# Kernel optimization log

Hardware: AMD Instinct MI355X
Metric: run time of the kernel (lower is better)

Reference implementation:

```python
import jax, jax.numpy as jnp
import numpy as np
from jax import lax

# Paraformer-large streaming decoder dims
L, H, DFF, NH, DK, K, V, T, S, CKV, LB = 16, 512, 2048, 4, 128, 11, 8404, 64, 2048, 256, 256


def _ln(x, g, b, eps=1e-5):
    m = jnp.mean(x, axis=-1, keepdims=True)
    var = jnp.mean((x - m) ** 2, axis=-1, keepdims=True)
    return (x - m) * lax.rsqrt(var + eps) * g + b


def setup_inputs() -> dict:
    key = jax.random.key(0)
    ks = jax.random.split(key, 20)
    w = lambda k, shp: jax.random.normal(k, shp, jnp.float32) * 0.02
    return {
        "encoder_out": jax.random.normal(ks[0], (1, S, H), jnp.float32),
        "list_frame": jax.random.normal(ks[1], (1, T, H), jnp.float32),
        "fsmn_cache": jax.random.normal(ks[2], (L, 1, H, K - 1), jnp.float32),
        "key_cache": jax.random.normal(ks[3], (L, NH, DK, CKV), jnp.float32),
        "value_cache": jax.random.normal(ks[4], (L, NH, CKV, DK), jnp.float32),
        "norm1_g": jnp.ones((L, H)), "norm1_b": jnp.zeros((L, H)),
        "norm2_g": jnp.ones((L, H)), "norm2_b": jnp.zeros((L, H)),
        "norm3_g": jnp.ones((L, H)), "norm3_b": jnp.zeros((L, H)),
        "ffn_norm_g": jnp.ones((L, DFF)), "ffn_norm_b": jnp.zeros((L, DFF)),
        "w1": w(ks[5], (L, H, DFF)), "b1": jnp.zeros((L, DFF)),
        "w2": w(ks[6], (L, DFF, H)),  # bias-free in FunASR DecoderSANM
        "fsmn_w": w(ks[7], (L, H, K)),  # depthwise conv, groups=H, no bias
        "qw": w(ks[8], (L, H, H)), "qb": jnp.zeros((L, H)),
        "kvw": w(ks[9], (L, H, 2 * H)), "kvb": jnp.zeros((L, 2 * H)),
        "ow": w(ks[10], (L, H, H)), "ob": jnp.zeros((L, H)),
        "d3_norm1_g": jnp.ones((H,)), "d3_norm1_b": jnp.zeros((H,)),
        "d3_w1": w(ks[11], (H, DFF)), "d3_b1": jnp.zeros((DFF,)),
        "d3_ffn_norm_g": jnp.ones((DFF,)), "d3_ffn_norm_b": jnp.zeros((DFF,)),
        "d3_w2": w(ks[12], (DFF, H)),
        "after_norm_g": jnp.ones((H,)), "after_norm_b": jnp.zeros((H,)),
        "out_w": w(ks[13], (H, V)), "out_b": jnp.zeros((V,)),
        "list_frame_len": T,
    }


def reference(encoder_out, list_frame, fsmn_cache, key_cache, value_cache,
              norm1_g, norm1_b, norm2_g, norm2_b, norm3_g, norm3_b,
              ffn_norm_g, ffn_norm_b, w1, b1, w2, fsmn_w, qw, qb, kvw, kvb, ow, ob,
              d3_norm1_g, d3_norm1_b, d3_w1, d3_b1, d3_ffn_norm_g, d3_ffn_norm_b, d3_w2,
              after_norm_g, after_norm_b, out_w, out_b, list_frame_len):
    enc = encoder_out[0]  # [S, H]
    scale = DK ** -0.5

    def layer_fn(lf, p):
        (fc, kc, vc, n1g, n1b, n2g, n2b, n3g, n3b, fng, fnb,
         W1, B1, W2, FW, QW, QB, KVW, KVB, OW, OB) = p
        residual = lf
        y = _ln(lf, n1g, n1b)
        y = _ln(jax.nn.relu(y @ W1 + B1), fng, fnb) @ W2
        y = _ln(y, n2g, n2b)
        # cache concat; slice [look_back:] with look_back = -(K-1)-T keeps all K-1+T cols
        x_cat = jnp.concatenate([fc, jnp.swapaxes(y, 1, 2)], axis=-1)  # [1, H, K-1+T]
        conv = lax.conv_general_dilated(
            x_cat, FW[:, None, :], (1,), 'VALID',
            dimension_numbers=('NCH', 'OIH', 'NCH'), feature_group_count=H)  # [1, H, T]
        x = jnp.swapaxes(conv, 1, 2) + y + residual
        residual = x
        q = (_ln(x, n3g, n3b)[0] @ QW + QB).reshape(-1, NH, DK).transpose(1, 0, 2) * scale  # [h, T, dk]
        kv = enc @ KVW + KVB  # [S, 2H]
        k = kv[:, :H].reshape(-1, NH, DK).transpose(1, 2, 0)  # [h, dk, S]
        v = kv[:, H:].reshape(-1, NH, DK).transpose(1, 0, 2)  # [h, S, dk]
        k = jnp.concatenate([kc, k], axis=2)  # [h, dk, CKV+S]
        v = jnp.concatenate([vc, v], axis=1)  # [h, CKV+S, dk]
        attn = jax.nn.softmax(jnp.einsum('htd,hds->hts', q, k), axis=-1)
        ctx = jnp.einsum('hts,hsd->htd', attn, v).transpose(1, 0, 2).reshape(1, -1, H)
        lf = residual + ctx @ OW + OB
        return lf, (x_cat, k[:, :, -LB:], v[:, -LB:, :])

    layer_params = (fsmn_cache, key_cache, value_cache, norm1_g, norm1_b, norm2_g, norm2_b,
                    norm3_g, norm3_b, ffn_norm_g, ffn_norm_b, w1, b1, w2, fsmn_w,
                    qw, qb, kvw, kvb, ow, ob)
    lf, (save_fsmn, save_keys, save_values) = lax.scan(layer_fn, list_frame, layer_params)
    x = _ln(lf, d3_norm1_g, d3_norm1_b)
    x = _ln(jax.nn.relu(x @ d3_w1 + d3_b1), d3_ffn_norm_g, d3_ffn_norm_b) @ d3_w2
    logits = _ln(x, after_norm_g, after_norm_b) @ out_w + out_b
    max_logit_ids = jnp.argmax(logits, axis=-1).astype(jnp.int32)
    return save_fsmn, save_keys, save_values, max_logit_ids
```

## Files before the change

kernel.cpp:

```cpp
#include <hip/hip_runtime.h>

constexpr int LAY = 16, HID = 512, FF = 2048, NHD = 4, DKH = 128, KW = 11,
              VOC = 8404, TT = 64, SEQ = 2048, LBN = 256;

#define SWZ(row, e) ((e) ^ ((((row) >> 2) & 7) << 2))

__global__ void diag_k(float* __restrict__ p, float v) { p[threadIdx.x] = v; }

__global__ __launch_bounds__(256) void redln_k(
    const float* __restrict__ P, int N, int nch,
    const float* __restrict__ bias, const float* __restrict__ res, int relu,
    const float* __restrict__ g, const float* __restrict__ b,
    float* __restrict__ out1, float* __restrict__ out2) {
  __shared__ float buf[2048];
  __shared__ float red[256];
  const int m = blockIdx.x, tid = threadIdx.x;
  float s = 0.f;
  for (int n = tid; n < N; n += 256) {
    const float* p = P + (size_t)m * N + n;
    float v = 0.f;
    for (int c = 0; c < nch; ++c) v += p[(size_t)c * 64 * N];
    if (bias) v += bias[n];
    if (res) v += res[(size_t)m * N + n];
    if (relu) v = fmaxf(v, 0.f);
    if (out1) out1[(size_t)m * N + n] = v;
    buf[n] = v; s += v;
  }
  red[tid] = s; __syncthreads();
  for (int st = 128; st > 0; st >>= 1) { if (tid < st) red[tid] += red[tid + st]; __syncthreads(); }
  const float mean = red[0] / N;
  __syncthreads();
  float vs = 0.f;
  for (int n = tid; n < N; n += 256) { float d = buf[n] - mean; vs += d * d; }
  red[tid] = vs; __syncthreads();
  for (int st = 128; st > 0; st >>= 1) { if (tid < st) red[tid] += red[tid + st]; __syncthreads(); }
  const float inv = rsqrtf(red[0] / N + 1e-5f);
  for (int n = tid; n < N; n += 256)
    out2[(size_t)m * N + n] = (buf[n] - mean) * inv * g[n] + b[n];
}

__global__ __launch_bounds__(256) void gemm32_nn(
    const float* __restrict__ A, int lda, long sA,
    const float* __restrict__ B, int ldb, long sB,
    int N, int Kd, int nch,
    float* __restrict__ part, long pzs, int coff,
    int aCh, long aChS) {
  __shared__ float As[64][64];
  __shared__ float Bs[64][40];
  const int tid = threadIdx.x;
  const int l16r = tid >> 4, l16c = tid & 15;
  const int lr = tid >> 3, lc = tid & 7;
  const int bn = blockIdx.x * 32;
  const int chunk = blockIdx.y;
  const int z = blockIdx.z;
  A += (long)z * sA; B += (long)z * sB;
  float acc[2][4] = {};
  const int ktiles = Kd >> 6;
  const int fa = (l16c & 7) << 2;
  for (int kt = chunk; kt < ktiles; kt += nch) {
    const int k0 = kt << 6;
    __syncthreads();
#pragma unroll
    for (int i = 0; i < 4; ++i) {
      const int r = l16r + 16 * i;
      const float* ap = A + (size_t)r * lda + k0 + l16c * 4;
      float4 av = *(const float4*)ap;
      for (int c = 1; c < aCh; ++c) {
        const float4 t2 = *(const float4*)(ap + (size_t)c * aChS);
        av.x += t2.x; av.y += t2.y; av.z += t2.z; av.w += t2.w;
      }
      As[l16c * 4 + 0][r ^ fa] = av.x; As[l16c * 4 + 1][r ^ fa] = av.y;
      As[l16c * 4 + 2][r ^ fa] = av.z; As[l16c * 4 + 3][r ^ fa] = av.w;
    }
#pragma unroll
    for (int i = 0; i < 2; ++i) {
      const int rb = lr + 32 * i;
      const float4 bv = *(const float4*)(B + (size_t)(k0 + rb) * ldb + bn + lc * 4);
      *(float4*)(&Bs[rb][lc * 4]) = bv;
    }
    __syncthreads();
#pragma unroll 8
    for (int kk = 0; kk < 64; ++kk) {
      const int fk = ((kk >> 2) & 7) << 2;
      const float2 a = *(const float2*)(&As[kk][(lr * 2) ^ fk]);
      const float4 b = *(const float4*)(&Bs[kk][lc * 4]);
      acc[0][0] += a.x * b.x; acc[0][1] += a.x * b.y; acc[0][2] += a.x * b.z; acc[0][3] += a.x * b.w;
      acc[1][0] += a.y * b.x; acc[1][1] += a.y * b.y; acc[1][2] += a.y * b.z; acc[1][3] += a.y * b.w;
    }
  }
  float* P = part + (size_t)z * pzs + (size_t)(coff + chunk) * 64 * N;
#pragma unroll
  for (int i = 0; i < 2; ++i) {
    const int m = lr * 2 + i;
#pragma unroll
    for (int j = 0; j < 4; ++j) P[(size_t)m * N + bn + lc * 4 + j] = acc[i][j];
  }
}

__global__ __launch_bounds__(256) void gemm_nn(
    const float* __restrict__ A, int lda, long sA,
    const float* __restrict__ B, int ldb, long sB,
    float* __restrict__ C, int ldc, long sC,
    const float* __restrict__ bias,
    const float* __restrict__ res, int ldres,
    int N, int Kd, int flags, int nch,
    float* __restrict__ part, long pzs, int coff,
    int aCh, long aChS) {
  __shared__ float As[64][64];
  __shared__ float Bs[64][64];
  const int tid = threadIdx.x;
  const int lr = tid >> 4, lc = tid & 15;
  const int bn = blockIdx.x * 64;
  const int chunk = blockIdx.y;
  const int z = blockIdx.z;
  A += (long)z * sA; B += (long)z * sB; C += (long)z * sC;
  float acc[4][4] = {};
  const int ktiles = Kd >> 6;
  const int fa = (lc & 7) << 2;
  for (int kt = chunk; kt < ktiles; kt += nch) {
    const int k0 = kt << 6;
    __syncthreads();
#pragma unroll
    for (int i = 0; i < 4; ++i) {
      const int r = lr + 16 * i;
      const float* ap = A + (size_t)r * lda + k0 + lc * 4;
      float4 av = *(const float4*)ap;
      for (int c = 1; c < aCh; ++c) {
        const float4 t2 = *(const float4*)(ap + (size_t)c * aChS);
        av.x += t2.x; av.y += t2.y; av.z += t2.z; av.w += t2.w;
      }
      As[lc * 4 + 0][r ^ fa] = av.x; As[lc * 4 + 1][r ^ fa] = av.y;
      As[lc * 4 + 2][r ^ fa] = av.z; As[lc * 4 + 3][r ^ fa] = av.w;
      const int n = bn + lc * 4;
      const float* bp = B + (size_t)(k0 + r) * ldb + n;
      float4 bv;
      if (n + 3 < N) bv = *(const float4*)bp;
      else {
        bv.x = (n + 0 < N) ? bp[0] : 0.f;
        bv.y = (n + 1 < N) ? bp[1] : 0.f;
        bv.z = (n + 2 < N) ? bp[2] : 0.f;
        bv.w = (n + 3 < N) ? bp[3] : 0.f;
      }
      *(float4*)(&Bs[r][SWZ(r, lc * 4)]) = bv;
    }
    __syncthreads();
#pragma unroll 8
    for (int kk = 0; kk < 64; ++kk) {
      const int fk = ((kk >> 2) & 7) << 2;
      const float4 a = *(const float4*)(&As[kk][(lr * 4) ^ fk]);
      const float4 b = *(const float4*)(&Bs[kk][(lc * 4) ^ fk]);
      acc[0][0] += a.x * b.x; acc[0][1] += a.x * b.y; acc[0][2] += a.x * b.z; acc[0][3] += a.x * b.w;
      acc[1][0] += a.y * b.x; acc[1][1] += a.y * b.y; acc[1][2] += a.y * b.z; acc[1][3] += a.y * b.w;
      acc[2][0] += a.z * b.x; acc[2][1] += a.z * b.y; acc[2][2] += a.z * b.z; acc[2][3] += a.z * b.w;
      acc[3][0] += a.w * b.x; acc[3][1] += a.w * b.y; acc[3][2] += a.w * b.z; acc[3][3] += a.w * b.w;
    }
  }
  if (part) {
    float* P = part + (size_t)z * pzs + (size_t)(coff + chunk) * 64 * N;
#pragma unroll
    for (int i = 0; i < 4; ++i) {
      const int m = lr * 4 + i;
#pragma unroll
      for (int j = 0; j < 4; ++j) P[(size_t)m * N + bn + lc * 4 + j] = acc[i][j];
    }
    return;
  }
#pragma unroll
  for (int i = 0; i < 4; ++i) {
    const int m = lr * 4 + i;
#pragma unroll
    for (int j = 0; j < 4; ++j) {
      const int n = bn + lc * 4 + j;
      if (n < N) {
        float v = acc[i][j];
        if (bias) v += bias[n];
        if (res) v += res[(size_t)m * ldres + n];
        if (flags & 2) v += C[(size_t)m * ldc + n];
        if (flags & 1) v = fmaxf(v, 0.f);
        C[(size_t)m * ldc + n] = v;
      }
    }
  }
}

__global__ __launch_bounds__(256) void red_k(
    const float* __restrict__ P, float* __restrict__ out,
    int N, int nch, long pzs, int outld, int zoff,
    const float* __restrict__ bias, const float* __restrict__ res,
    const float* __restrict__ rsv, const float* __restrict__ bvv,
    int relu, int total) {
  const int idx = blockIdx.x * 256 + threadIdx.x;
  if (idx >= total) return;
  const int z = idx / (64 * N);
  const int rem = idx - z * 64 * N;
  const int t = rem / N;
  const int n = rem - t * N;
  const float* p = P + (size_t)z * pzs + (size_t)t * N + n;
  float s = 0.f;
  for (int c = 0; c < nch; ++c) s += p[(size_t)c * 64 * N];
  const int oc = z * zoff + n;
  if (bias) s += bias[oc];
  if (res) s += res[(size_t)t * outld + oc];
  if (rsv) s += rsv[z * 64 + t] * bvv[oc];
  if (relu) s = fmaxf(s, 0.f);
  out[(size_t)t * outld + oc] = s;
}

__global__ __launch_bounds__(256) void gemm_nt(
    const float* __restrict__ A, int lda, long sA,
    const float* __restrict__ B, int ldb, long sB,
    float* __restrict__ C, int ldc, long sC,
    int N, int Kd, int nch, float* __restrict__ part) {
  __shared__ float As[64][64];
  __shared__ float Bs[64][64];
  const int tid = threadIdx.x;
  const int lr = tid >> 4, lc = tid & 15;
  const int bn = blockIdx.x * 64;
  const int chunk = blockIdx.y;
  const int z = blockIdx.z;
  A += (long)z * sA; B += (long)z * sB; C += (long)z * sC;
  float acc[4][4] = {};
  const int ktiles = Kd >> 6;
  const int fa = (lc & 7) << 2;
  for (int kt = chunk; kt < ktiles; kt += nch) {
    const int k0 = kt << 6;
    __syncthreads();
#pragma unroll
    for (int i = 0; i < 4; ++i) {
      const int r = lr + 16 * i;
      const float4 av = *(const float4*)(A + (size_t)r * lda + k0 + lc * 4);
      As[lc * 4 + 0][r ^ fa] = av.x; As[lc * 4 + 1][r ^ fa] = av.y;
      As[lc * 4 + 2][r ^ fa] = av.z; As[lc * 4 + 3][r ^ fa] = av.w;
      const float4 bv = *(const float4*)(B + (size_t)(bn + r) * ldb + k0 + lc * 4);
      Bs[lc * 4 + 0][r ^ fa] = bv.x; Bs[lc * 4 + 1][r ^ fa] = bv.y;
      Bs[lc * 4 + 2][r ^ fa] = bv.z; Bs[lc * 4 + 3][r ^ fa] = bv.w;
    }
    __syncthreads();
#pragma unroll 8
    for (int kk = 0; kk < 64; ++kk) {
      const int fk = ((kk >> 2) & 7) << 2;
      const float4 a = *(const float4*)(&As[kk][(lr * 4) ^ fk]);
      const float4 b = *(const float4*)(&Bs[kk][(lc * 4) ^ fk]);
      acc[0][0] += a.x * b.x; acc[0][1] += a.x * b.y; acc[0][2] += a.x * b.z; acc[0][3] += a.x * b.w;
      acc[1][0] += a.y * b.x; acc[1][1] += a.y * b.y; acc[1][2] += a.y * b.z; acc[1][3] += a.y * b.w;
      acc[2][0] += a.z * b.x; acc[2][1] += a.z * b.y; acc[2][2] += a.z * b.z; acc[2][3] += a.z * b.w;
      acc[3][0] += a.w * b.x; acc[3][1] += a.w * b.y; acc[3][2] += a.w * b.z; acc[3][3] += a.w * b.w;
    }
  }
  if (chunk == 0) {
#pragma unroll
    for (int i = 0; i < 4; ++i)
#pragma unroll
      for (int j = 0; j < 4; ++j)
        C[(size_t)(lr * 4 + i) * ldc + bn + lc * 4 + j] = acc[i][j];
  } else {
    float* P = part + (size_t)z * (64L * SEQ) + (size_t)(chunk - 1) * 64 * SEQ * NHD;
#pragma unroll
    for (int i = 0; i < 4; ++i)
#pragma unroll
      for (int j = 0; j < 4; ++j)
        P[(size_t)(lr * 4 + i) * SEQ + bn + lc * 4 + j] = acc[i][j];
  }
}

__global__ __launch_bounds__(256) void attn1_k(
    const float* __restrict__ qpart, const float* __restrict__ qbi_l,
    const float* __restrict__ Wkv, const float* __restrict__ kcl,
    float* __restrict__ qp, float* __restrict__ sc,
    int ckv, int sct) {
  __shared__ float As[64][64];
  __shared__ float Bs[64][64];
  const int tid = threadIdx.x;
  const int lr = tid >> 4, lc = tid & 15;
  const int h = blockIdx.z;
  const bool isQp = blockIdx.x < 8;
  const int bn = (isQp ? blockIdx.x : blockIdx.x - 8) * 64;
  const int fa = (lc & 7) << 2;
  float acc[4][4] = {};
  for (int k0 = 0; k0 < DKH; k0 += 64) {
    __syncthreads();
#pragma unroll
    for (int i = 0; i < 4; ++i) {
      const int r = lr + 16 * i;
      const float* ap = qpart + (size_t)r * HID + h * DKH + k0 + lc * 4;
      float4 av = *(const float4*)ap;
      for (int c = 1; c < 8; ++c) {
        const float4 t2 = *(const float4*)(ap + (size_t)c * 64 * HID);
        av.x += t2.x; av.y += t2.y; av.z += t2.z; av.w += t2.w;
      }
      const float4 bb = *(const float4*)(qbi_l + h * DKH + k0 + lc * 4);
      av.x += bb.x; av.y += bb.y; av.z += bb.z; av.w += bb.w;
      As[lc * 4 + 0][r ^ fa] = av.x; As[lc * 4 + 1][r ^ fa] = av.y;
      As[lc * 4 + 2][r ^ fa] = av.z; As[lc * 4 + 3][r ^ fa] = av.w;
      if (isQp) {
        const float4 bv = *(const float4*)(Wkv + (size_t)(bn + r) * (2 * HID) + h * DKH + k0 + lc * 4);
        Bs[lc * 4 + 0][r ^ fa] = bv.x; Bs[lc * 4 + 1][r ^ fa] = bv.y;
        Bs[lc * 4 + 2][r ^ fa] = bv.z; Bs[lc * 4 + 3][r ^ fa] = bv.w;
      } else {
        const float4 bv = *(const float4*)(kcl + ((size_t)h * DKH + k0 + r) * ckv + bn + lc * 4);
        *(float4*)(&Bs[r][SWZ(r, lc * 4)]) = bv;
      }
    }
    __syncthreads();
#pragma unroll 8
    for (int kk = 0; kk < 64; ++kk) {
      const int fk = ((kk >> 2) & 7) << 2;
      const float4 a = *(const float4*)(&As[kk][(lr * 4) ^ fk]);
      const float4 b = *(const float4*)(&Bs[kk][(lc * 4) ^ fk]);
      acc[0][0] += a.x * b.x; acc[0][1] += a.x * b.y; acc[0][2] += a.x * b.z; acc[0][3] += a.x * b.w;
      acc[1][0] += a.y * b.x; acc[1][1] += a.y * b.y; acc[1][2] += a.y * b.z; acc[1][3] += a.y * b.w;
      acc[2][0] += a.z * b.x; acc[2][1] += a.z * b.y; acc[2][2] += a.z * b.z; acc[2][3] += a.z * b.w;
      acc[3][0] += a.w * b.x; acc[3][1] += a.w * b.y; acc[3][2] += a.w * b.z; acc[3][3] += a.w * b.w;
    }
  }
  if (isQp) {
    float* C = qp + (size_t)h * TT * HID;
#pragma unroll
    for (int i = 0; i < 4; ++i)
#pragma unroll
      for (int j = 0; j < 4; ++j)
        C[(size_t)(lr * 4 + i) * HID + bn + lc * 4 + j] = acc[i][j];
  } else {
    float* C = sc + (size_t)h * TT * sct;
#pragma unroll
    for (int i = 0; i < 4; ++i)
#pragma unroll
      for (int j = 0; j < 4; ++j)
        C[(size_t)(lr * 4 + i) * sct + bn + lc * 4 + j] = acc[i][j];
  }
}

__global__ __launch_bounds__(256) void attn2_k(
    const float* __restrict__ sc, const float* __restrict__ vcl,
    const float* __restrict__ enc,
    float* __restrict__ part, float* __restrict__ partE,
    int ckv, int sct, int ncho, long pzc) {
  __shared__ float As[64][64];
  __shared__ float Bs[64][64];
  const int tid = threadIdx.x;
  const int lr = tid >> 4, lc = tid & 15;
  const int h = blockIdx.z;
  const int by = blockIdx.y;
  const bool isOld = blockIdx.x < 2;
  if (isOld && by >= ncho) return;
  if (!isOld && by >= 8) return;
  const float* A;
  const float* Bb;
  int lda, ldb, N, ktiles, nch, bn;
  float* P;
  if (isOld) {
    A = sc + (size_t)h * TT * sct;  lda = sct;
    Bb = vcl + (size_t)h * ckv * DKH; ldb = DKH;
    N = DKH; ktiles = ckv >> 6; nch = ncho; bn = blockIdx.x * 64;
    P = part + (size_t)h * pzc + (size_t)by * 64 * DKH;
  } else {
    A = sc + ckv + (size_t)h * TT * sct; lda = sct;
    Bb = enc; ldb = HID;
    N = HID; ktiles = SEQ >> 6; nch = 8; bn = (blockIdx.x - 2) * 64;
    P = partE + (size_t)h * (8L * 64 * HID) + (size_t)by * 64 * HID;
  }
  const int fa = (lc & 7) << 2;
  float acc[4][4] = {};
  for (int kt = by; kt < ktiles; kt += nch) {
    const int k0 = kt << 6;
    __syncthreads();
#pragma unroll
    for (int i = 0; i < 4; ++i) {
      const int r = lr + 16 * i;
      const float4 av = *(const float4*)(A + (size_t)r * lda + k0 + lc * 4);
      As[lc * 4 + 0][r ^ fa] = av.x; As[lc * 4 + 1][r ^ fa] = av.y;
      As[lc * 4 + 2][r ^ fa] = av.z; As[lc * 4 + 3][r ^ fa] = av.w;
      const float4 bv = *(const float4*)(Bb + (size_t)(k0 + r) * ldb + bn + lc * 4);
      *(float4*)(&Bs[r][SWZ(r, lc * 4)]) = bv;
    }
    __syncthreads();
#pragma unroll 8
    for (int kk = 0; kk < 64; ++kk) {
      const int fk = ((kk >> 2) & 7) << 2;
      const float4 a = *(const float4*)(&As[kk][(lr * 4) ^ fk]);
      const float4 b = *(const float4*)(&Bs[kk][(lc * 4) ^ fk]);
      acc[0][0] += a.x * b.x; acc[0][1] += a.x * b.y; acc[0][2] += a.x * b.z; acc[0][3] += a.x * b.w;
      acc[1][0] += a.y * b.x; acc[1][1] += a.y * b.y; acc[1][2] += a.y * b.z; acc[1][3] += a.y * b.w;
      acc[2][0] += a.z * b.x; acc[2][1] += a.z * b.y; acc[2][2] += a.z * b.z; acc[2][3] += a.z * b.w;
      acc[3][0] += a.w * b.x; acc[3][1] += a.w * b.y; acc[3][2] += a.w * b.z; acc[3][3] += a.w * b.w;
    }
  }
#pragma unroll
  for (int i = 0; i < 4; ++i)
#pragma unroll
    for (int j = 0; j < 4; ++j)
      P[(size_t)(lr * 4 + i) * N + bn + lc * 4 + j] = acc[i][j];
}

__global__ __launch_bounds__(256) void fsmnln_k(
    const float* __restrict__ y4, const float* __restrict__ lfin,
    const float* __restrict__ cache, const float* __restrict__ fw,
    const float* __restrict__ g, const float* __restrict__ b,
    float* __restrict__ xb, float* __restrict__ xcat,
    float* __restrict__ y1out) {
  __shared__ float buf[HID];
  __shared__ float red[256];
  const int t = blockIdx.x, tid = threadIdx.x;
  float s = 0.f;
  for (int h = tid; h < HID; h += 256) {
    float conv = 0.f;
#pragma unroll
    for (int k = 0; k < KW; ++k) {
      const int j = t + k;
      const float xcv = (j < KW - 1) ? cache[h * (KW - 1) + j]
                                     : y4[(size_t)(j - (KW - 1)) * HID + h];
      conv += xcv * fw[h * KW + k];
    }
    const float yv = y4[(size_t)t * HID + h];
    const float x = conv + yv + lfin[(size_t)t * HID + h];
    xb[(size_t)t * HID + h] = x;
    buf[h] = x; s += x;
    xcat[h * (KW - 1 + TT) + (KW - 1) + t] = yv;
    if (t == 0) {
      for (int j2 = 0; j2 < KW - 1; ++j2)
        xcat[h * (KW - 1 + TT) + j2] = cache[h * (KW - 1) + j2];
    }
  }
  red[tid] = s; __syncthreads();
  for (int st = 128; st > 0; st >>= 1) { if (tid < st) red[tid] += red[tid + st]; __syncthreads(); }
  const float mean = red[0] / HID;
  __syncthreads();
  float vs = 0.f;
  for (int h = tid; h < HID; h += 256) { float d = buf[h] - mean; vs += d * d; }
  red[tid] = vs; __syncthreads();
  for (int st = 128; st > 0; st >>= 1) { if (tid < st) red[tid] += red[tid + st]; __syncthreads(); }
  const float inv = rsqrtf(red[0] / HID + 1e-5f);
  for (int h = tid; h < HID; h += 256)
    y1out[(size_t)t * HID + h] = (buf[h] - mean) * inv * g[h] + b[h];
}

__global__ __launch_bounds__(256) void softmax_k(
    float* __restrict__ sc, float* __restrict__ rs,
    const float* __restrict__ qpart, const float* __restrict__ qbi_l,
    const float* __restrict__ kb, const float* __restrict__ partN,
    int cols, int newStart, float alpha) {
  __shared__ float srow[8192];
  __shared__ float red[256];
  const int tid = threadIdx.x;
  const int row = blockIdx.x;
  const int h = row >> 6, t = row & 63;
  sc += (size_t)row * cols;
  const float* pn = partN + (size_t)h * 64 * SEQ + (size_t)t * SEQ;
  float qv = 0.f;
  if (tid < DKH) {
    const float* qp0 = qpart + (size_t)t * HID + h * DKH + tid;
    float q = qp0[0];
    for (int c = 1; c < 8; ++c) q += qp0[(size_t)c * 64 * HID];
    q += qbi_l[h * DKH + tid];
    qv = q * kb[h * DKH + tid];
  }
  red[tid] = qv; __syncthreads();
  for (int st = 64; st > 0; st >>= 1) { if (tid < st) red[tid] += red[tid + st]; __syncthreads(); }
  const float qcv = red[0];
  __syncthreads();
  float m = -3.4e38f;
  for (int c = tid; c < cols; c += 256) {
    float v = sc[c];
    if (c >= newStart) v += pn[c - newStart] + qcv;
    v *= alpha;
    srow[c] = v; m = fmaxf(m, v);
  }
  red[tid] = m; __syncthreads();
  for (int st = 128; st > 0; st >>= 1) { if (tid < st) red[tid] = fmaxf(red[tid], red[tid + st]); __syncthreads(); }
  m = red[0]; __syncthreads();
  float s = 0.f;
  for (int c = tid; c < cols; c += 256) {
    const float e = __expf(srow[c] - m);
    srow[c] = e; s += e;
  }
  red[tid] = s; __syncthreads();
  for (int st = 128; st > 0; st >>= 1) { if (tid < st) red[tid] += red[tid + st]; __syncthreads(); }
  const float inv = 1.f / red[0];
  float ns = 0.f;
  for (int c = tid; c < cols; c += 256) {
    const float p = srow[c] * inv; sc[c] = p;
    if (c >= newStart) ns += p;
  }
  __syncthreads();
  red[tid] = ns; __syncthreads();
  for (int st = 128; st > 0; st >>= 1) { if (tid < st) red[tid] += red[tid + st]; __syncthreads(); }
  if (tid == 0) rs[row] = red[0];
}

__global__ __launch_bounds__(256) void argmax_k(const float* __restrict__ lg,
                                                float* __restrict__ out) {
  __shared__ float vs[256];
  __shared__ int ix[256];
  const int tid = threadIdx.x;
  lg += (size_t)blockIdx.x * VOC;
  float bm = -3.4e38f;
  int bi = 0;
  for (int c = tid; c < VOC; c += 256) { float v = lg[c]; if (v > bm) { bm = v; bi = c; } }
  vs[tid] = bm; ix[tid] = bi; __syncthreads();
  for (int st = 128; st > 0; st >>= 1) {
    if (tid < st) {
      if (vs[tid + st] > vs[tid] || (vs[tid + st] == vs[tid] && ix[tid + st] < ix[tid])) {
        vs[tid] = vs[tid + st]; ix[tid] = ix[tid + st];
      }
    }
    __syncthreads();
  }
  if (tid == 0) out[blockIdx.x] = (float)ix[0];
}

__global__ __launch_bounds__(256) void kvsave_k(const float* __restrict__ enc,
                                                const float* __restrict__ kvw,
                                                const float* __restrict__ kvb,
                                                float* __restrict__ keys,
                                                float* __restrict__ vals) {
  __shared__ float As[64][64];
  __shared__ float Bs[64][64];
  const int tid = threadIdx.x;
  const int lr = tid >> 4, lc = tid & 15;
  const int bn = blockIdx.x * 64, bm = blockIdx.y * 64;
  const int l = blockIdx.z;
  const float* W = kvw + (size_t)l * HID * 2 * HID;
  const int fa = (lc & 7) << 2;
  float acc[4][4] = {};
  for (int k0 = 0; k0 < HID; k0 += 64) {
    __syncthreads();
#pragma unroll
    for (int i = 0; i < 4; ++i) {
      const int r = lr + 16 * i;
      const float4 av =
          *(const float4*)(enc + (size_t)(SEQ - LBN + bm + r) * HID + k0 + lc * 4);
      As[lc * 4 + 0][r ^ fa] = av.x; As[lc * 4 + 1][r ^ fa] = av.y;
      As[lc * 4 + 2][r ^ fa] = av.z; As[lc * 4 + 3][r ^ fa] = av.w;
      const float4 bv = *(const float4*)(W + (size_t)(k0 + r) * (2 * HID) + bn + lc * 4);
      *(float4*)(&Bs[r][SWZ(r, lc * 4)]) = bv;
    }
    __syncthreads();
#pragma unroll 8
    for (int kk = 0; kk < 64; ++kk) {
      const int fk = ((kk >> 2) & 7) << 2;
      const float4 a = *(const float4*)(&As[kk][(lr * 4) ^ fk]);
      const float4 b = *(const float4*)(&Bs[kk][(lc * 4) ^ fk]);
      acc[0][0] += a.x * b.x; acc[0][1] += a.x * b.y; acc[0][2] += a.x * b.z; acc[0][3] += a.x * b.w;
      acc[1][0] += a.y * b.x; acc[1][1] += a.y * b.y; acc[1][2] += a.y * b.z; acc[1][3] += a.y * b.w;
      acc[2][0] += a.z * b.x; acc[2][1] += a.z * b.y; acc[2][2] += a.z * b.z; acc[2][3] += a.z * b.w;
      acc[3][0] += a.w * b.x; acc[3][1] += a.w * b.y; acc[3][2] += a.w * b.z; acc[3][3] += a.w * b.w;
    }
  }
#pragma unroll
  for (int i = 0; i < 4; ++i) {
    const int m = bm + lr * 4 + i;
#pragma unroll
    for (int j = 0; j < 4; ++j) {
      const int n = bn + lc * 4 + j;
      const float v = acc[i][j] + kvb[(size_t)l * 2 * HID + n];
      if (n < 512) {
        const int h = n >> 7, d = n & 127;
        keys[(((size_t)l * NHD + h) * DKH + d) * LBN + m] = v;
      } else {
        const int c = n - 512, h = c >> 7, d = c & 127;
        vals[(((size_t)l * NHD + h) * LBN + m) * DKH + d] = v;
      }
    }
  }
}

extern "C" void kernel_launch(void* const* d_in, const int* in_sizes, int n_in,
                              void* d_out, int out_size, void* d_ws, size_t ws_size,
                              hipStream_t stream) {
  static const int EXPECT[34] = {
      1048576, 32768, 81920, -1, -1,
      8192, 8192, 8192, 8192, 8192, 8192,
      32768, 32768,
      16777216, 32768, 16777216, 90112,
      4194304, 8192, 8388608, 16384, 4194304, 8192,
      512, 512, 1048576, 2048, 2048, 2048, 1048576,
      512, 512, 4302848, 8404};
  if (out_size != 4800576) {
    diag_k<<<1, 64, 0, stream>>>((float*)d_out, 9800000.f);
    return;
  }
  float* out_fsmn = (float*)d_out;
  float* out_keys = out_fsmn + (size_t)LAY * HID * (KW - 1 + TT);
  float* out_vals = out_keys + (size_t)LAY * NHD * DKH * LBN;
  float* out_ids  = out_vals + (size_t)LAY * NHD * LBN * DKH;
  if (n_in < 34) {
    diag_k<<<1, 64, 0, stream>>>(out_ids, 9900000.f);
    return;
  }
  for (int i = 0; i < 34; ++i) {
    if (EXPECT[i] >= 0 && in_sizes[i] != EXPECT[i]) {
      diag_k<<<1, 64, 0, stream>>>(out_ids, (float)((i + 1) * 100000));
      return;
    }
  }
  const long per = (long)LAY * NHD * DKH;
  const long ckl = (long)in_sizes[3] / per;
  if ((long)in_sizes[3] != ckl * per || in_sizes[4] != in_sizes[3] ||
      ckl <= 0 || (ckl & 63) != 0 || ckl > 6144) {
    diag_k<<<1, 64, 0, stream>>>(out_fsmn, (float)in_sizes[3]);
    return;
  }
  if (ws_size < (size_t)3145728 * 4) {
    diag_k<<<1, 64, 0, stream>>>(out_fsmn, 1.0e6f + (float)(ws_size >> 20));
    return;
  }
  const int ckv = (int)ckl;
  const int sct = ckv + SEQ;
  const long TS = (long)TT * sct;
  const int ncho = (ckv / 64 < 8) ? (ckv / 64) : 8;

  const float* enc    = (const float*)d_in[0];
  const float* lfrm   = (const float*)d_in[1];
  const float* fcache = (const float*)d_in[2];
  const float* kcache = (const float*)d_in[3];
  const float* vcache = (const float*)d_in[4];
  const float* n1g = (const float*)d_in[5];  const float* n1b = (const float*)d_in[6];
  const float* n2g = (const float*)d_in[7];  const float* n2b = (const float*)d_in[8];
  const float* n3g = (const float*)d_in[9];  const float* n3b = (const float*)d_in[10];
  const float* fng = (const float*)d_in[11]; const float* fnb = (const float*)d_in[12];
  const float* w1  = (const float*)d_in[13]; const float* b1  = (const float*)d_in[14];
  const float* w2  = (const float*)d_in[15];
  const float* fw  = (const float*)d_in[16];
  const float* qw  = (const float*)d_in[17]; const float* qbi  = (const float*)d_in[18];
  const float* kvw = (const float*)d_in[19]; const float* kvbi = (const float*)d_in[20];
  const float* ow  = (const float*)d_in[21]; const float* obi  = (const float*)d_in[22];
  const float* d3n1g = (const float*)d_in[23]; const float* d3n1b = (const float*)d_in[24];
  const float* d3w1  = (const float*)d_in[25]; const float* d3b1  = (const float*)d_in[26];
  const float* d3fng = (const float*)d_in[27]; const float* d3fnb = (const float*)d_in[28];
  const float* d3w2  = (const float*)d_in[29];
  const float* ang   = (const float*)d_in[30]; const float* anb = (const float*)d_in[31];
  const float* outw  = (const float*)d_in[32]; const float* outb = (const float*)d_in[33];

  float* sc  = out_keys;
  float* ov  = out_vals;
  float* lf  = ov + 0;
  float* y1  = ov + 32768;
  float* y4  = ov + 98304;
  float* xb  = ov + 131072;
  float* ctx = ov + 196608;
  float* y2  = ov + 360448;
  float* qp  = ov + 491520;
  float* rs  = ov + 753920;
  float* lg  = ov + 754176;
  float* wsf   = (float*)d_ws;
  float* part  = wsf;
  float* partE = wsf + 1048576;
  float* partN = wsf + 2097152;

  const float alpha = 0.08838834764831845f;
  const long TH = (long)TT * HID;
  const long pz_ctx = (long)(ncho + 4) * 64 * DKH;

  redln_k<<<TT, 256, 0, stream>>>(lfrm, HID, 1, nullptr, nullptr, 0,
                                  n1g, n1b, lf, y1);

  for (int l = 0; l < LAY; ++l) {
    const float* Wkv = kvw + (size_t)l * HID * 2 * HID;
    const float* Bkv = kvbi + (size_t)l * 2 * HID;
    const float* qbi_l = qbi + (size_t)l * HID;
    gemm32_nn<<<dim3(64, 8, 1), 256, 0, stream>>>(
        y1, HID, 0, w1 + (size_t)l * HID * FF, FF, 0, FF, HID, 8, part, 0, 0, 1, 0);
    redln_k<<<TT, 256, 0, stream>>>(part, FF, 8, b1 + (size_t)l * FF, nullptr, 1,
                                    fng + (size_t)l * FF, fnb + (size_t)l * FF,
                                    nullptr, y2);
    gemm32_nn<<<dim3(16, 32, 1), 256, 0, stream>>>(
        y2, FF, 0, w2 + (size_t)l * FF * HID, HID, 0, HID, FF, 32, part, 0, 0, 1, 0);
    redln_k<<<TT, 256, 0, stream>>>(part, HID, 32, nullptr, nullptr, 0,
                                    n2g + l * HID, n2b + l * HID, nullptr, y4);
    fsmnln_k<<<TT, 256, 0, stream>>>(y4, lf, fcache + (size_t)l * HID * (KW - 1),
                                     fw + (size_t)l * HID * KW,
                                     n3g + l * HID, n3b + l * HID,
                                     xb, out_fsmn + (size_t)l * HID * (KW - 1 + TT), y1);
    gemm32_nn<<<dim3(16, 8, 1), 256, 0, stream>>>(
        y1, HID, 0, qw + (size_t)l * HID * HID, HID, 0, HID, HID, 8, part, 0, 0, 1, 0);
    attn1_k<<<dim3(8 + ckv / 64, 1, NHD), 256, 0, stream>>>(
        part, qbi_l, Wkv, kcache + (size_t)l * NHD * DKH * ckv, qp, sc, ckv, sct);
    gemm_nt<<<dim3(32, 2, NHD), 256, 0, stream>>>(
        qp, HID, TH, enc, HID, 0, sc + ckv, sct, TS, SEQ, HID, 2, partN);
    softmax_k<<<NHD * TT, 256, 0, stream>>>(sc, rs, part, qbi_l, Bkv, partN,
                                            sct, ckv, alpha);
    attn2_k<<<dim3(10, 8, NHD), 256, 0, stream>>>(
        sc, vcache + (size_t)l * NHD * ckv * DKH, enc, part, partE,
        ckv, sct, ncho, pz_ctx);
    gemm32_nn<<<dim3(4, 4, NHD), 256, 0, stream>>>(
        partE, HID, 8L * 64 * HID, Wkv + HID, 2 * HID, DKH, DKH, HID, 4,
        part, pz_ctx, ncho, 8, 64L * HID);
    red_k<<<128, 256, 0, stream>>>(part, ctx, DKH, ncho + 4, pz_ctx, HID, DKH,
                                   nullptr, nullptr, rs, Bkv + HID, 0, NHD * TT * DKH);
    gemm32_nn<<<dim3(16, 8, 1), 256, 0, stream>>>(
        ctx, HID, 0, ow + (size_t)l * HID * HID, HID, 0, HID, HID, 8, part, 0, 0, 1, 0);
    const float* ng = (l + 1 < LAY) ? n1g + (l + 1) * HID : d3n1g;
    const float* nb = (l + 1 < LAY) ? n1b + (l + 1) * HID : d3n1b;
    redln_k<<<TT, 256, 0, stream>>>(part, HID, 8, obi + (size_t)l * HID, xb, 0,
                                    ng, nb, lf, y1);
  }

  gemm32_nn<<<dim3(64, 8, 1), 256, 0, stream>>>(
      y1, HID, 0, d3w1, FF, 0, FF, HID, 8, part, 0, 0, 1, 0);
  redln_k<<<TT, 256, 0, stream>>>(part, FF, 8, d3b1, nullptr, 1,
                                  d3fng, d3fnb, nullptr, y2);
  gemm32_nn<<<dim3(16, 32, 1), 256, 0, stream>>>(
      y2, FF, 0, d3w2, HID, 0, HID, FF, 32, part, 0, 0, 1, 0);
  redln_k<<<TT, 256, 0, stream>>>(part, HID, 32, nullptr, nullptr, 0,
                                  ang, anb, nullptr, y4);
  gemm_nn<<<dim3((VOC + 63) / 64, 1, 1), 256, 0, stream>>>(
      y4, HID, 0, outw, VOC, 0, lg, VOC, 0, outb, nullptr, 0,
      VOC, HID, 0, 1, nullptr, 0, 0, 1, 0);
  argmax_k<<<TT, 256, 0, stream>>>(lg, out_ids);

  kvsave_k<<<dim3(2 * HID / 64, LBN / 64, LAY), 256, 0, stream>>>(
      enc, kvw, kvbi, out_keys, out_vals);
}
```

Baseline: 2.944 ms.

## Fuse the whole decoder chain into one cooperative persistent kernel

Replaces the roughly 200 per-layer kernel launches with a single cooperative kernel that runs every stage as a grid-strided device function, with grid-wide barriers between stages. The fallback path keeps separate launches of the same device functions. This targets launch overhead and inter-kernel gaps in a latency-bound small-batch decoder. In exchange it adds grid.sync costs and caps the grid at 512 blocks, which can reduce parallelism in some stages.

```diff
diff --git a/kernel.cpp b/kernel.cpp
--- a/kernel.cpp
+++ b/kernel.cpp
@@ -1,4 +1,7 @@
 #include <hip/hip_runtime.h>
+#include <hip/hip_cooperative_groups.h>
+
+namespace cg = cooperative_groups;
 
 constexpr int LAY = 16, HID = 512, FF = 2048, NHD = 4, DKH = 128, KW = 11,
               VOC = 8404, TT = 64, SEQ = 2048, LBN = 256;
@@ -6,432 +9,633 @@
 #define SWZ(row, e) ((e) ^ ((((row) >> 2) & 7) << 2))
 
 __global__ void diag_k(float* __restrict__ p, float v) { p[threadIdx.x] = v; }
+
+struct CA {
+  const float* enc; const float* lfrm; const float* fcache;
+  const float* kcache; const float* vcache;
+  const float* n1g; const float* n1b; const float* n2g; const float* n2b;
+  const float* n3g; const float* n3b; const float* fng; const float* fnb;
+  const float* w1; const float* b1; const float* w2; const float* fw;
+  const float* qw; const float* qbi; const float* kvw; const float* kvbi;
+  const float* ow; const float* obi;
+  const float* d3n1g; const float* d3n1b; const float* d3w1; const float* d3b1;
+  const float* d3fng; const float* d3fnb; const float* d3w2;
+  const float* ang; const float* anb; const float* outw; const float* outb;
+  float* lf; float* y1; float* y2; float* y4; float* xb; float* ctx;
+  float* rs; float* lg; float* sc;
+  float* part; float* partE; float* partN;
+  float* out_fsmn; float* out_ids;
+  int ckv; int sct; int ncho; long pz_ctx;
+};
+
+__device__ void d_redln(const float* __restrict__ P, int N, int nch,
+                        const float* __restrict__ bias,
+                        const float* __restrict__ res, int relu,
+                        const float* __restrict__ g, const float* __restrict__ b,
+                        float* __restrict__ out1, float* __restrict__ out2,
+                        float* sm) {
+  float* buf = sm;
+  float* red = sm + 2048;
+  const int tid = threadIdx.x;
+  for (int m = blockIdx.x; m < 64; m += gridDim.x) {
+    float s = 0.f;
+    for (int n = tid; n < N; n += 256) {
+      const float* p = P + (size_t)m * N + n;
+      float v = 0.f;
+      for (int c = 0; c < nch; ++c) v += p[(size_t)c * 64 * N];
+      if (bias) v += bias[n];
+      if (res) v += res[(size_t)m * N + n];
+      if (relu) v = fmaxf(v, 0.f);
+      if (out1) out1[(size_t)m * N + n] = v;
+      buf[n] = v; s += v;
+    }
+    red[tid] = s; __syncthreads();
+    for (int st = 128; st > 0; st >>= 1) { if (tid < st) red[tid] += red[tid + st]; __syncthreads(); }
+    const float mean = red[0] / N;
+    __syncthreads();
+    float vs = 0.f;
+    for (int n = tid; n < N; n += 256) { float d = buf[n] - mean; vs += d * d; }
+    red[tid] = vs; __syncthreads();
+    for (int st = 128; st > 0; st >>= 1) { if (tid < st) red[tid] += red[tid + st]; __syncthreads(); }
+    const float inv = rsqrtf(red[0] / N + 1e-5f);
+    for (int n = tid; n < N; n += 256)
+      out2[(size_t)m * N + n] = (buf[n] - mean) * inv * g[n] + b[n];
+    __syncthreads();
+  }
+}
+
+__device__ void d_gemm32(const float* __restrict__ A, int lda, long sA,
+                         const float* __restrict__ B, int ldb, long sB,
+                         int N, int Kd, int nch, int Z,
+                         float* __restrict__ part, long pzs, int coff,
+                         int aCh, long aChS, float* sm) {
+  const int nx = N >> 5;
+  const int tot = nx * nch * Z;
+  const int tid = threadIdx.x;
+  const int l16r = tid >> 4, l16c = tid & 15;
+  const int lr = tid >> 3, lc = tid & 7;
+  float (*As)[64] = (float(*)[64])sm;
+  float (*Bs)[40] = (float(*)[40])(sm + 4096);
+  const int fa = (l16c & 7) << 2;
+  const int ktiles = Kd >> 6;
+  for (int vb = blockIdx.x; vb < tot; vb += gridDim.x) {
+    const int bx = vb % nx;
+    const int r2 = vb / nx;
+    const int chunk = r2 % nch;
+    const int z = r2 / nch;
+    const float* Az = A + (long)z * sA;
+    const float* Bz = B + (long)z * sB;
+    const int bn = bx * 32;
+    float acc[2][4] = {};
+    for (int kt = chunk; kt < ktiles; kt += nch) {
+      const int k0 = kt << 6;
+      __syncthreads();
+#pragma unroll
+      for (int i = 0; i < 4; ++i) {
+        const int r = l16r + 16 * i;
+        const float* ap = Az + (size_t)r * lda + k0 + l16c * 4;
+        float4 av = *(const float4*)ap;
+        for (int c = 1; c < aCh; ++c) {
+          const float4 t2 = *(const float4*)(ap + (size_t)c * aChS);
+          av.x += t2.x; av.y += t2.y; av.z += t2.z; av.w += t2.w;
+        }
+        As[l16c * 4 + 0][r ^ fa] = av.x; As[l16c * 4 + 1][r ^ fa] = av.y;
+        As[l16c * 4 + 2][r ^ fa] = av.z; As[l16c * 4 + 3][r ^ fa] = av.w;
+      }
+#pragma unroll
+      for (int i = 0; i < 2; ++i) {
+        const int rb = lr + 32 * i;
+        const float4 bv = *(const float4*)(Bz + (size_t)(k0 + rb) * ldb + bn + lc * 4);
+        *(float4*)(&Bs[rb][lc * 4]) = bv;
+      }
+      __syncthreads();
+#pragma unroll 8
+      for (int kk = 0; kk < 64; ++kk) {
+        const int fk = ((kk >> 2) & 7) << 2;
+        const float2 aa = *(const float2*)(&As[kk][(lr * 2) ^ fk]);
+        const float4 bb = *(const float4*)(&Bs[kk][lc * 4]);
+        acc[0][0] += aa.x * bb.x; acc[0][1] += aa.x * bb.y; acc[0][2] += aa.x * bb.z; acc[0][3] += aa.x * bb.w;
+        acc[1][0] += aa.y * bb.x; acc[1][1] += aa.y * bb.y; acc[1][2] += aa.y * bb.z; acc[1][3] += aa.y * bb.w;
+      }
+    }
+    float* P = part + (size_t)z * pzs + (size_t)(coff + chunk) * 64 * N;
+#pragma unroll
+    for (int i = 0; i < 2; ++i) {
+      const int m = lr * 2 + i;
+#pragma unroll
+      for (int j = 0; j < 4; ++j) P[(size_t)m * N + bn + lc * 4 + j] = acc[i][j];
+    }
+    __syncthreads();
+  }
+}
+
+__device__ void d_fsmnln(const float* __restrict__ y4, const float* __restrict__ lfin,
+                         const float* __restrict__ cache, const float* __restrict__ fw,
+                         const float* __restrict__ g, const float* __restrict__ b,
+                         float* __restrict__ xb, float* __restrict__ xcat,
+                         float* __restrict__ y1out, float* sm) {
+  float* buf = sm;
+  float* red = sm + 512;
+  const int tid = threadIdx.x;
+  for (int t = blockIdx.x; t < 64; t += gridDim.x) {
+    float s = 0.f;
+    for (int h = tid; h < HID; h += 256) {
+      float conv = 0.f;
+#pragma unroll
+      for (int k = 0; k < KW; ++k) {
+        const int j = t + k;
+        const float xcv = (j < KW - 1) ? cache[h * (KW - 1) + j]
+                                       : y4[(size_t)(j - (KW - 1)) * HID + h];
+        conv += xcv * fw[h * KW + k];
+      }
+      const float yv = y4[(size_t)t * HID + h];
+      const float x = conv + yv + lfin[(size_t)t * HID + h];
+      xb[(size_t)t * HID + h] = x;
+      buf[h] = x; s += x;
+      xcat[h * (KW - 1 + TT) + (KW - 1) + t] = yv;
+      if (t == 0) {
+        for (int j2 = 0; j2 < KW - 1; ++j2)
+          xcat[h * (KW - 1 + TT) + j2] = cache[h * (KW - 1) + j2];
+      }
+    }
+    red[tid] = s; __syncthreads();
+    for (int st = 128; st > 0; st >>= 1) { if (tid < st) red[tid] += red[tid + st]; __syncthreads(); }
+    const float mean = red[0] / HID;
+    __syncthreads();
+    float vs = 0.f;
+    for (int h = tid; h < HID; h += 256) { float d = buf[h] - mean; vs += d * d; }
+    red[tid] = vs; __syncthreads();
+    for (int st = 128; st > 0; st >>= 1) { if (tid < st) red[tid] += red[tid + st]; __syncthreads(); }
+    const float inv = rsqrtf(red[0] / HID + 1e-5f);
+    for (int h = tid; h < HID; h += 256)
+      y1out[(size_t)t * HID + h] = (buf[h] - mean) * inv * g[h] + b[h];
+    __syncthreads();
+  }
+}
+
+__device__ void d_attn1(const float* __restrict__ qpart, const float* __restrict__ qbi_l,
+                        const float* __restrict__ Wkv, const float* __restrict__ kcl,
+                        float* __restrict__ qp, float* __restrict__ sc,
+                        int ckv, int sct, float* sm) {
+  const int nx = 8 + ckv / 64;
+  const int tot = nx * NHD;
+  const int tid = threadIdx.x;
+  const int lr = tid >> 4, lc = tid & 15;
+  float (*As)[64] = (float(*)[64])sm;
+  float (*Bs)[64] = (float(*)[64])(sm + 4096);
+  const int fa = (lc & 7) << 2;
+  for (int vb = blockIdx.x; vb < tot; vb += gridDim.x) {
+    const int bxx = vb % nx;
+    const int h = vb / nx;
+    const bool isQp = bxx < 8;
+    const int bn = (isQp ? bxx : bxx - 8) * 64;
+    float acc[4][4] = {};
+    for (int k0 = 0; k0 < DKH; k0 += 64) {
+      __syncthreads();
+#pragma unroll
+      for (int i = 0; i < 4; ++i) {
+        const int r = lr + 16 * i;
+        const float* ap = qpart + (size_t)r * HID + h * DKH + k0 + lc * 4;
+        float4 av = *(const float4*)ap;
+        for (int c = 1; c < 8; ++c) {
+          const float4 t2 = *(const float4*)(ap + (size_t)c * 64 * HID);
+          av.x += t2.x; av.y += t2.y; av.z += t2.z; av.w += t2.w;
+        }
+        const float4 bb = *(const float4*)(qbi_l + h * DKH + k0 + lc * 4);
+        av.x += bb.x; av.y += bb.y; av.z += bb.z; av.w += bb.w;
+        As[lc * 4 + 0][r ^ fa] = av.x; As[lc * 4 + 1][r ^ fa] = av.y;
+        As[lc * 4 + 2][r ^ fa] = av.z; As[lc * 4 + 3][r ^ fa] = av.w;
+        if (isQp) {
+          const float4 bv = *(const float4*)(Wkv + (size_t)(bn + r) * (2 * HID) + h * DKH + k0 + lc * 4);
+          Bs[lc * 4 + 0][r ^ fa] = bv.x; Bs[lc * 4 + 1][r ^ fa] = bv.y;
+          Bs[lc * 4 + 2][r ^ fa] = bv.z; Bs[lc * 4 + 3][r ^ fa] = bv.w;
+        } else {
+          const float4 bv = *(const float4*)(kcl + ((size_t)h * DKH + k0 + r) * ckv + bn + lc * 4);
+          *(float4*)(&Bs[r][SWZ(r, lc * 4)]) = bv;
+        }
+      }
+      __syncthreads();
+#pragma unroll 8
+      for (int kk = 0; kk < 64; ++kk) {
+        const int fk = ((kk >> 2) & 7) << 2;
+        const float4 a = *(const float4*)(&As[kk][(lr * 4) ^ fk]);
+        const float4 b = *(const float4*)(&Bs[kk][(lc * 4) ^ fk]);
+        acc[0][0] += a.x * b.x; acc[0][1] += a.x * b.y; acc[0][2] += a.x * b.z; acc[0][3] += a.x * b.w;
+        acc[1][0] += a.y * b.x; acc[1][1] += a.y * b.y; acc[1][2] += a.y * b.z; acc[1][3] += a.y * b.w;
+        acc[2][0] += a.z * b.x; acc[2][1] += a.z * b.y; acc[2][2] += a.z * b.z; acc[2][3] += a.z * b.w;
+        acc[3][0] += a.w * b.x; acc[3][1] += a.w * b.y; acc[3][2] += a.w * b.z; acc[3][3] += a.w * b.w;
+      }
+    }
+    if (isQp) {
+      float* C = qp + (size_t)h * TT * HID;
+#pragma unroll
+      for (int i = 0; i < 4; ++i)
+#pragma unroll
+        for (int j = 0; j < 4; ++j)
+          C[(size_t)(lr * 4 + i) * HID + bn + lc * 4 + j] = acc[i][j];
+    } else {
+      float* C = sc + (size_t)h * TT * sct;
+#pragma unroll
+      for (int i = 0; i < 4; ++i)
+#pragma unroll
+        for (int j = 0; j < 4; ++j)
+          C[(size_t)(lr * 4 + i) * sct + bn + lc * 4 + j] = acc[i][j];
+    }
+    __syncthreads();
+  }
+}
+
+__device__ void d_scnew(const float* __restrict__ qp, const float* __restrict__ enc,
+                        float* __restrict__ sc, float* __restrict__ partN,
+                        int ckv, int sct, float* sm) {
+  const int tot = 32 * 2 * NHD;
+  const int tid = threadIdx.x;
+  const int lr = tid >> 4, lc = tid & 15;
+  float (*As)[64] = (float(*)[64])sm;
+  float (*Bs)[64] = (float(*)[64])(sm + 4096);
+  const int fa = (lc & 7) << 2;
+  const long TH = (long)TT * HID;
+  const long TS = (long)TT * sct;
+  for (int vb = blockIdx.x; vb < tot; vb += gridDim.x) {
+    const int bxx = vb & 31;
+    const int r2 = vb >> 5;
+    const int chunk = r2 & 1;
+    const int z = r2 >> 1;
+    const float* A = qp + (long)z * TH;
+    const int bn = bxx * 64;
+    float acc[4][4] = {};
+    for (int kt = chunk; kt < 8; kt += 2) {
+      const int k0 = kt << 6;
+      __syncthreads();
+#pragma unroll
+      for (int i = 0; i < 4; ++i) {
+        const int r = lr + 16 * i;
+        const float4 av = *(const float4*)(A + (size_t)r * HID + k0 + lc * 4);
+        As[lc * 4 + 0][r ^ fa] = av.x; As[lc * 4 + 1][r ^ fa] = av.y;
+        As[lc * 4 + 2][r ^ fa] = av.z; As[lc * 4 + 3][r ^ fa] = av.w;
+        const float4 bv = *(const float4*)(enc + (size_t)(bn + r) * HID + k0 + lc * 4);
+        Bs[lc * 4 + 0][r ^ fa] = bv.x; Bs[lc * 4 + 1][r ^ fa] = bv.y;
+        Bs[lc * 4 + 2][r ^ fa] = bv.z; Bs[lc * 4 + 3][r ^ fa] = bv.w;
+      }
+      __syncthreads();
+#pragma unroll 8
+      for (int kk = 0; kk < 64; ++kk) {
+        const int fk = ((kk >> 2) & 7) << 2;
+        const float4 a = *(const float4*)(&As[kk][(lr * 4) ^ fk]);
+        const float4 b = *(const float4*)(&Bs[kk][(lc * 4) ^ fk]);
+        acc[0][0] += a.x * b.x; acc[0][1] += a.x * b.y; acc[0][2] += a.x * b.z; acc[0][3] += a.x * b.w;
+        acc[1][0] += a.y * b.x; acc[1][1] += a.y * b.y; acc[1][2] += a.y * b.z; acc[1][3] += a.y * b.w;
+        acc[2][0] += a.z * b.x; acc[2][1] += a.z * b.y; acc[2][2] += a.z * b.z; acc[2][3] += a.z * b.w;
+        acc[3][0] += a.w * b.x; acc[3][1] += a.w * b.y; acc[3][2] += a.w * b.z; acc[3][3] += a.w * b.w;
+      }
+    }
+    if (chunk == 0) {
+      float* C = sc + ckv + (long)z * TS;
+#pragma unroll
+      for (int i = 0; i < 4; ++i)
+#pragma unroll
+        for (int j = 0; j < 4; ++j)
+          C[(size_t)(lr * 4 + i) * sct + bn + lc * 4 + j] = acc[i][j];
+    } else {
+      float* P = partN + (size_t)z * (64L * SEQ);
+#pragma unroll
+      for (int i = 0; i < 4; ++i)
+#pragma unroll
+        for (int j = 0; j < 4; ++j)
+          P[(size_t)(lr * 4 + i) * SEQ + bn + lc * 4 + j] = acc[i][j];
+    }
+    __syncthreads();
+  }
+}
+
+__device__ void d_softmax(float* __restrict__ sc, float* __restrict__ rs,
+                          const float* __restrict__ qpart, const float* __restrict__ qbi_l,
+                          const float* __restrict__ kb, const float* __restrict__ partN,
+                          int cols, int newStart, float alpha, float* sm) {
+  float* srow = sm;
+  float* red = sm + 8192;
+  const int tid = threadIdx.x;
+  for (int row = blockIdx.x; row < NHD * TT; row += gridDim.x) {
+    const int h = row >> 6, t = row & 63;
+    float* scr = sc + (size_t)row * cols;
+    const float* pn = partN + (size_t)h * 64 * SEQ + (size_t)t * SEQ;
+    float qv = 0.f;
+    if (tid < DKH) {
+      const float* qp0 = qpart + (size_t)t * HID + h * DKH + tid;
+      float q = qp0[0];
+      for (int c = 1; c < 8; ++c) q += qp0[(size_t)c * 64 * HID];
+      q += qbi_l[h * DKH + tid];
+      qv = q * kb[h * DKH + tid];
+    }
+    red[tid] = qv; __syncthreads();
+    for (int st = 64; st > 0; st >>= 1) { if (tid < st) red[tid] += red[tid + st]; __syncthreads(); }
+    const float qcv = red[0];
+    __syncthreads();
+    float m = -3.4e38f;
+    for (int c = tid; c < cols; c += 256) {
+      float v = scr[c];
+      if (c >= newStart) v += pn[c - newStart] + qcv;
+      v *= alpha;
+      srow[c] = v; m = fmaxf(m, v);
+    }
+    red[tid] = m; __syncthreads();
+    for (int st = 128; st > 0; st >>= 1) { if (tid < st) red[tid] = fmaxf(red[tid], red[tid + st]); __syncthreads(); }
+    m = red[0]; __syncthreads();
+    float s = 0.f;
+    for (int c = tid; c < cols; c += 256) {
+      const float e = __expf(srow[c] - m);
+      srow[c] = e; s += e;
+    }
+    red[tid] = s; __syncthreads();
+    for (int st = 128; st > 0; st >>= 1) { if (tid < st) red[tid] += red[tid + st]; __syncthreads(); }
+    const float inv = 1.f / red[0];
+    float ns = 0.f;
+    for (int c = tid; c < cols; c += 256) {
+      const float p = srow[c] * inv; scr[c] = p;
+      if (c >= newStart) ns += p;
+    }
+    __syncthreads();
+    red[tid] = ns; __syncthreads();
+    for (int st = 128; st > 0; st >>= 1) { if (tid < st) red[tid] += red[tid + st]; __syncthreads(); }
+    if (tid == 0) rs[row] = red[0];
+    __syncthreads();
+  }
+}
+
+__device__ void d_attn2(const float* __restrict__ sc, const float* __restrict__ vcl,
+                        const float* __restrict__ enc,
+                        float* __restrict__ part, float* __restrict__ partE,
+                        int ckv, int sct, int ncho, long pzc, float* sm) {
+  const int tot = 10 * 8 * NHD;
+  const int tid = threadIdx.x;
+  const int lr = tid >> 4, lc = tid & 15;
+  float (*As)[64] = (float(*)[64])sm;
+  float (*Bs)[64] = (float(*)[64])(sm + 4096);
+  const int fa = (lc & 7) << 2;
+  for (int vb = blockIdx.x; vb < tot; vb += gridDim.x) {
+    const int bxx = vb % 10;
+    const int r2 = vb / 10;
+    const int by = r2 % 8;
+    const int h = r2 / 8;
+    const bool isOld = bxx < 2;
+    if (isOld && by >= ncho) continue;
+    const float* A;
+    const float* Bb;
+    int lda, ldb, N, ktiles, nch, bn;
+    float* P;
+    if (isOld) {
+      A = sc + (size_t)h * TT * sct;  lda = sct;
+      Bb = vcl + (size_t)h * ckv * DKH; ldb = DKH;
+      N = DKH; ktiles = ckv >> 6; nch = ncho; bn = bxx * 64;
+      P = part + (size_t)h * pzc + (size_t)by * 64 * DKH;
+    } else {
+      A = sc + ckv + (size_t)h * TT * sct; lda = sct;
+      Bb = enc; ldb = HID;
+      N = HID; ktiles = SEQ >> 6; nch = 8; bn = (bxx - 2) * 64;
+      P = partE + (size_t)h * (8L * 64 * HID) + (size_t)by * 64 * HID;
+    }
+    float acc[4][4] = {};
+    for (int kt = by; kt < ktiles; kt += nch) {
+      const int k0 = kt << 6;
+      __syncthreads();
+#pragma unroll
+      for (int i = 0; i < 4; ++i) {
+        const int r = lr + 16 * i;
+        const float4 av = *(const float4*)(A + (size_t)r * lda + k0 + lc * 4);
+        As[lc * 4 + 0][r ^ fa] = av.x; As[lc * 4 + 1][r ^ fa] = av.y;
+        As[lc * 4 + 2][r ^ fa] = av.z; As[lc * 4 + 3][r ^ fa] = av.w;
+        const float4 bv = *(const float4*)(Bb + (size_t)(k0 + r) * ldb + bn + lc * 4);
+        *(float4*)(&Bs[r][SWZ(r, lc * 4)]) = bv;
+      }
+      __syncthreads();
+#pragma unroll 8
+      for (int kk = 0; kk < 64; ++kk) {
+        const int fk = ((kk >> 2) & 7) << 2;
+        const float4 a = *(const float4*)(&As[kk][(lr * 4) ^ fk]);
+        const float4 b = *(const float4*)(&Bs[kk][(lc * 4) ^ fk]);
+        acc[0][0] += a.x * b.x; acc[0][1] += a.x * b.y; acc[0][2] += a.x * b.z; acc[0][3] += a.x * b.w;
+        acc[1][0] += a.y * b.x; acc[1][1] += a.y * b.y; acc[1][2] += a.y * b.z; acc[1][3] += a.y * b.w;
+        acc[2][0] += a.z * b.x; acc[2][1] += a.z * b.y; acc[2][2] += a.z * b.z; acc[2][3] += a.z * b.w;
+        acc[3][0] += a.w * b.x; acc[3][1] += a.w * b.y; acc[3][2] += a.w * b.z; acc[3][3] += a.w * b.w;
+      }
+    }
+#pragma unroll
+    for (int i = 0; i < 4; ++i)
+#pragma unroll
+      for (int j = 0; j < 4; ++j)
+        P[(size_t)(lr * 4 + i) * N + bn + lc * 4 + j] = acc[i][j];
+    __syncthreads();
+  }
+}
+
+__device__ void d_red(const float* __restrict__ P, float* __restrict__ out,
+                      int N, int nch, long pzs, int outld, int zoff,
+                      const float* __restrict__ rsv, const float* __restrict__ bvv,
+                      int total) {
+  for (int idx = blockIdx.x * 256 + threadIdx.x; idx < total; idx += gridDim.x * 256) {
+    const int z = idx / (64 * N);
+    const int rem = idx - z * 64 * N;
+    const int t = rem / N;
+    const int n = rem - t * N;
+    const float* p = P + (size_t)z * pzs + (size_t)t * N + n;
+    float s = 0.f;
+    for (int c = 0; c < nch; ++c) s += p[(size_t)c * 64 * N];
+    const int oc = z * zoff + n;
+    s += rsv[z * 64 + t] * bvv[oc];
+    out[(size_t)t * outld + oc] = s;
+  }
+}
+
+__device__ void d_vocab(const float* __restrict__ A, const float* __restrict__ B,
+                        float* __restrict__ C, const float* __restrict__ bias,
+                        float* sm) {
+  const int tot = (VOC + 63) / 64;
+  const int tid = threadIdx.x;
+  const int lr = tid >> 4, lc = tid & 15;
+  float (*As)[64] = (float(*)[64])sm;
+  float (*Bs)[64] = (float(*)[64])(sm + 4096);
+  const int fa = (lc & 7) << 2;
+  for (int vb = blockIdx.x; vb < tot; vb += gridDim.x) {
+    const int bn = vb * 64;
+    float acc[4][4] = {};
+    for (int k0 = 0; k0 < HID; k0 += 64) {
+      __syncthreads();
+#pragma unroll
+      for (int i = 0; i < 4; ++i) {
+        const int r = lr + 16 * i;
+        const float4 av = *(const float4*)(A + (size_t)r * HID + k0 + lc * 4);
+        As[lc * 4 + 0][r ^ fa] = av.x; As[lc * 4 + 1][r ^ fa] = av.y;
+        As[lc * 4 + 2][r ^ fa] = av.z; As[lc * 4 + 3][r ^ fa] = av.w;
+        const int n = bn + lc * 4;
+        const float* bp = B + (size_t)(k0 + r) * VOC + n;
+        float4 bv;
+        if (n + 3 < VOC) bv = *(const float4*)bp;
+        else {
+          bv.x = (n + 0 < VOC) ? bp[0] : 0.f;
+          bv.y = (n + 1 < VOC) ? bp[1] : 0.f;
+          bv.z = (n + 2 < VOC) ? bp[2] : 0.f;
+          bv.w = (n + 3 < VOC) ? bp[3] : 0.f;
+        }
+        *(float4*)(&Bs[r][SWZ(r, lc * 4)]) = bv;
+      }
+      __syncthreads();
+#pragma unroll 8
+      for (int kk = 0; kk < 64; ++kk) {
+        const int fk = ((kk >> 2) & 7) << 2;
+        const float4 a = *(const float4*)(&As[kk][(lr * 4) ^ fk]);
+        const float4 b = *(const float4*)(&Bs[kk][(lc * 4) ^ fk]);
+        acc[0][0] += a.x * b.x; acc[0][1] += a.x * b.y; acc[0][2] += a.x * b.z; acc[0][3] += a.x * b.w;
+        acc[1][0] += a.y * b.x; acc[1][1] += a.y * b.y; acc[1][2] += a.y * b.z; acc[1][3] += a.y * b.w;
+        acc[2][0] += a.z * b.x; acc[2][1] += a.z * b.y; acc[2][2] += a.z * b.z; acc[2][3] += a.z * b.w;
+        acc[3][0] += a.w * b.x; acc[3][1] += a.w * b.y; acc[3][2] += a.w * b.z; acc[3][3] += a.w * b.w;
+      }
+    }
+#pragma unroll
+    for (int i = 0; i < 4; ++i) {
+      const int m = lr * 4 + i;
+#pragma unroll
+      for (int j = 0; j < 4; ++j) {
+        const int n = bn + lc * 4 + j;
+        if (n < VOC) C[(size_t)m * VOC + n] = acc[i][j] + bias[n];
+      }
+    }
+    __syncthreads();
+  }
+}
+
+__device__ void d_argmax(const float* __restrict__ lg, float* __restrict__ out,
+                         float* sm) {
+  float* vs = sm;
+  int* ix = (int*)(sm + 256);
+  const int tid = threadIdx.x;
+  for (int row = blockIdx.x; row < TT; row += gridDim.x) {
+    const float* lr_ = lg + (size_t)row * VOC;
+    float bm = -3.4e38f;
+    int bi = 0;
+    for (int c = tid; c < VOC; c += 256) { float v = lr_[c]; if (v > bm) { bm = v; bi = c; } }
+    vs[tid] = bm; ix[tid] = bi; __syncthreads();
+    for (int st = 128; st > 0; st >>= 1) {
+      if (tid < st) {
+        if (vs[tid + st] > vs[tid] || (vs[tid + st] == vs[tid] && ix[tid + st] < ix[tid])) {
+          vs[tid] = vs[tid + st]; ix[tid] = ix[tid + st];
+        }
+      }
+      __syncthreads();
+    }
+    if (tid == 0) out[row] = (float)ix[0];
+    __syncthreads();
+  }
+}
+
+__global__ __launch_bounds__(256, 2) void chain_k(CA a) {
+  __shared__ float sm[8448];
+  cg::grid_group grid = cg::this_grid();
+  const float alpha = 0.08838834764831845f;
+
+  d_redln(a.lfrm, HID, 1, nullptr, nullptr, 0, a.n1g, a.n1b, a.lf, a.y1, sm);
+  grid.sync();
+
+  for (int l = 0; l < LAY; ++l) {
+    const float* Wkv = a.kvw + (size_t)l * HID * 2 * HID;
+    const float* Bkv = a.kvbi + (size_t)l * 2 * HID;
+    const float* qbi_l = a.qbi + (size_t)l * HID;
+    d_gemm32(a.y1, HID, 0, a.w1 + (size_t)l * HID * FF, FF, 0, FF, HID, 8, 1,
+             a.part, 0, 0, 1, 0, sm);
+    grid.sync();
+    d_redln(a.part, FF, 8, a.b1 + (size_t)l * FF, nullptr, 1,
+            a.fng + (size_t)l * FF, a.fnb + (size_t)l * FF, nullptr, a.y2, sm);
+    grid.sync();
+    d_gemm32(a.y2, FF, 0, a.w2 + (size_t)l * FF * HID, HID, 0, HID, FF, 32, 1,
+             a.part, 0, 0, 1, 0, sm);
+    grid.sync();
+    d_redln(a.part, HID, 32, nullptr, nullptr, 0,
+            a.n2g + l * HID, a.n2b + l * HID, nullptr, a.y4, sm);
+    grid.sync();
+    d_fsmnln(a.y4, a.lf, a.fcache + (size_t)l * HID * (KW - 1),
+             a.fw + (size_t)l * HID * KW, a.n3g + l * HID, a.n3b + l * HID,
+             a.xb, a.out_fsmn + (size_t)l * HID * (KW - 1 + TT), a.y1, sm);
+    grid.sync();
+    d_gemm32(a.y1, HID, 0, a.qw + (size_t)l * HID * HID, HID, 0, HID, HID, 8, 1,
+             a.part, 0, 0, 1, 0, sm);
+    grid.sync();
+    d_attn1(a.part, qbi_l, Wkv, a.kcache + (size_t)l * NHD * DKH * a.ckv,
+            a.ctx, a.sc, a.ckv, a.sct, sm);
+    grid.sync();
+    d_scnew(a.ctx, a.enc, a.sc, a.partN, a.ckv, a.sct, sm);
+    grid.sync();
+    d_softmax(a.sc, a.rs, a.part, qbi_l, Bkv, a.partN, a.sct, a.ckv, alpha, sm);
+    grid.sync();
+    d_attn2(a.sc, a.vcache + (size_t)l * NHD * a.ckv * DKH, a.enc,
+            a.part, a.partE, a.ckv, a.sct, a.ncho, a.pz_ctx, sm);
+    grid.sync();
+    d_gemm32(a.partE, HID, 8L * 64 * HID, Wkv + HID, 2 * HID, DKH,
+             DKH, HID, 4, NHD, a.part, a.pz_ctx, a.ncho, 8, 64L * HID, sm);
+    grid.sync();
+    d_red(a.part, a.y2, DKH, a.ncho + 4, a.pz_ctx, HID, DKH,
+          a.rs, Bkv + HID, NHD * TT * DKH);
+    grid.sync();
+    d_gemm32(a.y2, HID, 0, a.ow + (size_t)l * HID * HID, HID, 0, HID, HID, 8, 1,
+             a.part, 0, 0, 1, 0, sm);
+    grid.sync();
+    const float* ng = (l + 1 < LAY) ? a.n1g + (l + 1) * HID : a.d3n1g;
+    const float* nb = (l + 1 < LAY) ? a.n1b + (l + 1) * HID : a.d3n1b;
+    d_redln(a.part, HID, 8, a.obi + (size_t)l * HID, a.xb, 0, ng, nb, a.lf, a.y1, sm);
+    grid.sync();
+  }
+
+  d_gemm32(a.y1, HID, 0, a.d3w1, FF, 0, FF, HID, 8, 1, a.part, 0, 0, 1, 0, sm);
+  grid.sync();
+  d_redln(a.part, FF, 8, a.d3b1, nullptr, 1, a.d3fng, a.d3fnb, nullptr, a.y2, sm);
+  grid.sync();
+  d_gemm32(a.y2, FF, 0, a.d3w2, HID, 0, HID, FF, 32, 1, a.part, 0, 0, 1, 0, sm);
+  grid.sync();
+  d_redln(a.part, HID, 32, nullptr, nullptr, 0, a.ang, a.anb, nullptr, a.y4, sm);
+  grid.sync();
+  d_vocab(a.y4, a.outw, a.lg, a.outb, sm);
+  grid.sync();
+  d_argmax(a.lg, a.out_ids, sm);
+}
 
 __global__ __launch_bounds__(256) void redln_k(
     const float* __restrict__ P, int N, int nch,
     const float* __restrict__ bias, const float* __restrict__ res, int relu,
     const float* __restrict__ g, const float* __restrict__ b,
     float* __restrict__ out1, float* __restrict__ out2) {
-  __shared__ float buf[2048];
-  __shared__ float red[256];
-  const int m = blockIdx.x, tid = threadIdx.x;
-  float s = 0.f;
-  for (int n = tid; n < N; n += 256) {
-    const float* p = P + (size_t)m * N + n;
-    float v = 0.f;
-    for (int c = 0; c < nch; ++c) v += p[(size_t)c * 64 * N];
-    if (bias) v += bias[n];
-    if (res) v += res[(size_t)m * N + n];
-    if (relu) v = fmaxf(v, 0.f);
-    if (out1) out1[(size_t)m * N + n] = v;
-    buf[n] = v; s += v;
-  }
-  red[tid] = s; __syncthreads();
-  for (int st = 128; st > 0; st >>= 1) { if (tid < st) red[tid] += red[tid + st]; __syncthreads(); }
-  const float mean = red[0] / N;
-  __syncthreads();
-  float vs = 0.f;
-  for (int n = tid; n < N; n += 256) { float d = buf[n] - mean; vs += d * d; }
-  red[tid] = vs; __syncthreads();
-  for (int st = 128; st > 0; st >>= 1) { if (tid < st) red[tid] += red[tid + st]; __syncthreads(); }
-  const float inv = rsqrtf(red[0] / N + 1e-5f);
-  for (int n = tid; n < N; n += 256)
-    out2[(size_t)m * N + n] = (buf[n] - mean) * inv * g[n] + b[n];
-}
-
-__global__ __launch_bounds__(256) void gemm32_nn(
+  __shared__ float sm[2304];
+  d_redln(P, N, nch, bias, res, relu, g, b, out1, out2, sm);
+}
+
+__global__ __launch_bounds__(256) void gemm32_k(
     const float* __restrict__ A, int lda, long sA,
     const float* __restrict__ B, int ldb, long sB,
-    int N, int Kd, int nch,
-    float* __restrict__ part, long pzs, int coff,
-    int aCh, long aChS) {
-  __shared__ float As[64][64];
-  __shared__ float Bs[64][40];
-  const int tid = threadIdx.x;
-  const int l16r = tid >> 4, l16c = tid & 15;
-  const int lr = tid >> 3, lc = tid & 7;
-  const int bn = blockIdx.x * 32;
-  const int chunk = blockIdx.y;
-  const int z = blockIdx.z;
-  A += (long)z * sA; B += (long)z * sB;
-  float acc[2][4] = {};
-  const int ktiles = Kd >> 6;
-  const int fa = (l16c & 7) << 2;
-  for (int kt = chunk; kt < ktiles; kt += nch) {
-    const int k0 = kt << 6;
-    __syncthreads();
-#pragma unroll
-    for (int i = 0; i < 4; ++i) {
-      const int r = l16r + 16 * i;
-      const float* ap = A + (size_t)r * lda + k0 + l16c * 4;
-      float4 av = *(const float4*)ap;
-      for (int c = 1; c < aCh; ++c) {
-        const float4 t2 = *(const float4*)(ap + (size_t)c * aChS);
-        av.x += t2.x; av.y += t2.y; av.z += t2.z; av.w += t2.w;
-      }
-      As[l16c * 4 + 0][r ^ fa] = av.x; As[l16c * 4 + 1][r ^ fa] = av.y;
-      As[l16c * 4 + 2][r ^ fa] = av.z; As[l16c * 4 + 3][r ^ fa] = av.w;
-    }
-#pragma unroll
-    for (int i = 0; i < 2; ++i) {
-      const int rb = lr + 32 * i;
-      const float4 bv = *(const float4*)(B + (size_t)(k0 + rb) * ldb + bn + lc * 4);
-      *(float4*)(&Bs[rb][lc * 4]) = bv;
-    }
-    __syncthreads();
-#pragma unroll 8
-    for (int kk = 0; kk < 64; ++kk) {
-      const int fk = ((kk >> 2) & 7) << 2;
-      const float2 a = *(const float2*)(&As[kk][(lr * 2) ^ fk]);
-      const float4 b = *(const float4*)(&Bs[kk][lc * 4]);
-      acc[0][0] += a.x * b.x; acc[0][1] += a.x * b.y; acc[0][2] += a.x * b.z; acc[0][3] += a.x * b.w;
-      acc[1][0] += a.y * b.x; acc[1][1] += a.y * b.y; acc[1][2] += a.y * b.z; acc[1][3] += a.y * b.w;
-    }
-  }
-  float* P = part + (size_t)z * pzs + (size_t)(coff + chunk) * 64 * N;
-#pragma unroll
-  for (int i = 0; i < 2; ++i) {
-    const int m = lr * 2 + i;
-#pragma unroll
-    for (int j = 0; j < 4; ++j) P[(size_t)m * N + bn + lc * 4 + j] = acc[i][j];
-  }
-}
-
-__global__ __launch_bounds__(256) void gemm_nn(
-    const float* __restrict__ A, int lda, long sA,
-    const float* __restrict__ B, int ldb, long sB,
-    float* __restrict__ C, int ldc, long sC,
-    const float* __restrict__ bias,
-    const float* __restrict__ res, int ldres,
-    int N, int Kd, int flags, int nch,
-    float* __restrict__ part, long pzs, int coff,
-    int aCh, long aChS) {
-  __shared__ float As[64][64];
-  __shared__ float Bs[64][64];
-  const int tid = threadIdx.x;
-  const int lr = tid >> 4, lc = tid & 15;
-  const int bn = blockIdx.x * 64;
-  const int chunk = blockIdx.y;
-  const int z = blockIdx.z;
-  A += (long)z * sA; B += (long)z * sB; C += (long)z * sC;
-  float acc[4][4] = {};
-  const int ktiles = Kd >> 6;
-  const int fa = (lc & 7) << 2;
-  for (int kt = chunk; kt < ktiles; kt += nch) {
-    const int k0 = kt << 6;
-    __syncthreads();
-#pragma unroll
-    for (int i = 0; i < 4; ++i) {
-      const int r = lr + 16 * i;
-      const float* ap = A + (size_t)r * lda + k0 + lc * 4;
-      float4 av = *(const float4*)ap;
-      for (int c = 1; c < aCh; ++c) {
-        const float4 t2 = *(const float4*)(ap + (size_t)c * aChS);
-        av.x += t2.x; av.y += t2.y; av.z += t2.z; av.w += t2.w;
-      }
-      As[lc * 4 + 0][r ^ fa] = av.x; As[lc * 4 + 1][r ^ fa] = av.y;
-      As[lc * 4 + 2][r ^ fa] = av.z; As[lc * 4 + 3][r ^ fa] = av.w;
-      const int n = bn + lc * 4;
-      const float* bp = B + (size_t)(k0 + r) * ldb + n;
-      float4 bv;
-      if (n + 3 < N) bv = *(const float4*)bp;
-      else {
-        bv.x = (n + 0 < N) ? bp[0] : 0.f;
-        bv.y = (n + 1 < N) ? bp[1] : 0.f;
-        bv.z = (n + 2 < N) ? bp[2] : 0.f;
-        bv.w = (n + 3 < N) ? bp[3] : 0.f;
-      }
-      *(float4*)(&Bs[r][SWZ(r, lc * 4)]) = bv;
-    }
-    __syncthreads();
-#pragma unroll 8
-    for (int kk = 0; kk < 64; ++kk) {
-      const int fk = ((kk >> 2) & 7) << 2;
-      const float4 a = *(const float4*)(&As[kk][(lr * 4) ^ fk]);
-      const float4 b = *(const float4*)(&Bs[kk][(lc * 4) ^ fk]);
-      acc[0][0] += a.x * b.x; acc[0][1] += a.x * b.y; acc[0][2] += a.x * b.z; acc[0][3] += a.x * b.w;
-      acc[1][0] += a.y * b.x; acc[1][1] += a.y * b.y; acc[1][2] += a.y * b.z; acc[1][3] += a.y * b.w;
-      acc[2][0] += a.z * b.x; acc[2][1] += a.z * b.y; acc[2][2] += a.z * b.z; acc[2][3] += a.z * b.w;
-      acc[3][0] += a.w * b.x; acc[3][1] += a.w * b.y; acc[3][2] += a.w * b.z; acc[3][3] += a.w * b.w;
-    }
-  }
-  if (part) {
-    float* P = part + (size_t)z * pzs + (size_t)(coff + chunk) * 64 * N;
-#pragma unroll
-    for (int i = 0; i < 4; ++i) {
-      const int m = lr * 4 + i;
-#pragma unroll
-      for (int j = 0; j < 4; ++j) P[(size_t)m * N + bn + lc * 4 + j] = acc[i][j];
-    }
-    return;
-  }
-#pragma unroll
-  for (int i = 0; i < 4; ++i) {
-    const int m = lr * 4 + i;
-#pragma unroll
-    for (int j = 0; j < 4; ++j) {
-      const int n = bn + lc * 4 + j;
-      if (n < N) {
-        float v = acc[i][j];
-        if (bias) v += bias[n];
-        if (res) v += res[(size_t)m * ldres + n];
-        if (flags & 2) v += C[(size_t)m * ldc + n];
-        if (flags & 1) v = fmaxf(v, 0.f);
-        C[(size_t)m * ldc + n] = v;
-      }
-    }
-  }
-}
-
-__global__ __launch_bounds__(256) void red_k(
-    const float* __restrict__ P, float* __restrict__ out,
-    int N, int nch, long pzs, int outld, int zoff,
-    const float* __restrict__ bias, const float* __restrict__ res,
-    const float* __restrict__ rsv, const float* __restrict__ bvv,
-    int relu, int total) {
-  const int idx = blockIdx.x * 256 + threadIdx.x;
-  if (idx >= total) return;
-  const int z = idx / (64 * N);
-  const int rem = idx - z * 64 * N;
-  const int t = rem / N;
-  const int n = rem - t * N;
-  const float* p = P + (size_t)z * pzs + (size_t)t * N + n;
-  float s = 0.f;
-  for (int c = 0; c < nch; ++c) s += p[(size_t)c * 64 * N];
-  const int oc = z * zoff + n;
-  if (bias) s += bias[oc];
-  if (res) s += res[(size_t)t * outld + oc];
-  if (rsv) s += rsv[z * 64 + t] * bvv[oc];
-  if (relu) s = fmaxf(s, 0.f);
-  out[(size_t)t * outld + oc] = s;
-}
-
-__global__ __launch_bounds__(256) void gemm_nt(
-    const float* __restrict__ A, int lda, long sA,
-    const float* __restrict__ B, int ldb, long sB,
-    float* __restrict__ C, int ldc, long sC,
-    int N, int Kd, int nch, float* __restrict__ part) {
-  __shared__ float As[64][64];
-  __shared__ float Bs[64][64];
-  const int tid = threadIdx.x;
-  const int lr = tid >> 4, lc = tid & 15;
-  const int bn = blockIdx.x * 64;
-  const int chunk = blockIdx.y;
-  const int z = blockIdx.z;
-  A += (long)z * sA; B += (long)z * sB; C += (long)z * sC;
-  float acc[4][4] = {};
-  const int ktiles = Kd >> 6;
-  const int fa = (lc & 7) << 2;
-  for (int kt = chunk; kt < ktiles; kt += nch) {
-    const int k0 = kt << 6;
-    __syncthreads();
-#pragma unroll
-    for (int i = 0; i < 4; ++i) {
-      const int r = lr + 16 * i;
-      const float4 av = *(const float4*)(A + (size_t)r * lda + k0 + lc * 4);
-      As[lc * 4 + 0][r ^ fa] = av.x; As[lc * 4 + 1][r ^ fa] = av.y;
-      As[lc * 4 + 2][r ^ fa] = av.z; As[lc * 4 + 3][r ^ fa] = av.w;
-      const float4 bv = *(const float4*)(B + (size_t)(bn + r) * ldb + k0 + lc * 4);
-      Bs[lc * 4 + 0][r ^ fa] = bv.x; Bs[lc * 4 + 1][r ^ fa] = bv.y;
-      Bs[lc * 4 + 2][r ^ fa] = bv.z; Bs[lc * 4 + 3][r ^ fa] = bv.w;
-    }
-    __syncthreads();
-#pragma unroll 8
-    for (int kk = 0; kk < 64; ++kk) {
-      const int fk = ((kk >> 2) & 7) << 2;
-      const float4 a = *(const float4*)(&As[kk][(lr * 4) ^ fk]);
-      const float4 b = *(const float4*)(&Bs[kk][(lc * 4) ^ fk]);
-      acc[0][0] += a.x * b.x; acc[0][1] += a.x * b.y; acc[0][2] += a.x * b.z; acc[0][3] += a.x * b.w;
-      acc[1][0] += a.y * b.x; acc[1][1] += a.y * b.y; acc[1][2] += a.y * b.z; acc[1][3] += a.y * b.w;
-      acc[2][0] += a.z * b.x; acc[2][1] += a.z * b.y; acc[2][2] += a.z * b.z; acc[2][3] += a.z * b.w;
-      acc[3][0] += a.w * b.x; acc[3][1] += a.w * b.y; acc[3][2] += a.w * b.z; acc[3][3] += a.w * b.w;
-    }
-  }
-  if (chunk == 0) {
-#pragma unroll
-    for (int i = 0; i < 4; ++i)
-#pragma unroll
-      for (int j = 0; j < 4; ++j)
-        C[(size_t)(lr * 4 + i) * ldc + bn + lc * 4 + j] = acc[i][j];
-  } else {
-    float* P = part + (size_t)z * (64L * SEQ) + (size_t)(chunk - 1) * 64 * SEQ * NHD;
-#pragma unroll
-    for (int i = 0; i < 4; ++i)
-#pragma unroll
-      for (int j = 0; j < 4; ++j)
-        P[(size_t)(lr * 4 + i) * SEQ + bn + lc * 4 + j] = acc[i][j];
-  }
-}
-
-__global__ __launch_bounds__(256) void attn1_k(
-    const float* __restrict__ qpart, const float* __restrict__ qbi_l,
-    const float* __restrict__ Wkv, const float* __restrict__ kcl,
-    float* __restrict__ qp, float* __restrict__ sc,
-    int ckv, int sct) {
-  __shared__ float As[64][64];
-  __shared__ float Bs[64][64];
-  const int tid = threadIdx.x;
-  const int lr = tid >> 4, lc = tid & 15;
-  const int h = blockIdx.z;
-  const bool isQp = blockIdx.x < 8;
-  const int bn = (isQp ? blockIdx.x : blockIdx.x - 8) * 64;
-  const int fa = (lc & 7) << 2;
-  float acc[4][4] = {};
-  for (int k0 = 0; k0 < DKH; k0 += 64) {
-    __syncthreads();
-#pragma unroll
-    for (int i = 0; i < 4; ++i) {
-      const int r = lr + 16 * i;
-      const float* ap = qpart + (size_t)r * HID + h * DKH + k0 + lc * 4;
-      float4 av = *(const float4*)ap;
-      for (int c = 1; c < 8; ++c) {
-        const float4 t2 = *(const float4*)(ap + (size_t)c * 64 * HID);
-        av.x += t2.x; av.y += t2.y; av.z += t2.z; av.w += t2.w;
-      }
-      const float4 bb = *(const float4*)(qbi_l + h * DKH + k0 + lc * 4);
-      av.x += bb.x; av.y += bb.y; av.z += bb.z; av.w += bb.w;
-      As[lc * 4 + 0][r ^ fa] = av.x; As[lc * 4 + 1][r ^ fa] = av.y;
-      As[lc * 4 + 2][r ^ fa] = av.z; As[lc * 4 + 3][r ^ fa] = av.w;
-      if (isQp) {
-        const float4 bv = *(const float4*)(Wkv + (size_t)(bn + r) * (2 * HID) + h * DKH + k0 + lc * 4);
-        Bs[lc * 4 + 0][r ^ fa] = bv.x; Bs[lc * 4 + 1][r ^ fa] = bv.y;
-        Bs[lc * 4 + 2][r ^ fa] = bv.z; Bs[lc * 4 + 3][r ^ fa] = bv.w;
-      } else {
-        const float4 bv = *(const float4*)(kcl + ((size_t)h * DKH + k0 + r) * ckv + bn + lc * 4);
-        *(float4*)(&Bs[r][SWZ(r, lc * 4)]) = bv;
-      }
-    }
-    __syncthreads();
-#pragma unroll 8
-    for (int kk = 0; kk < 64; ++kk) {
-      const int fk = ((kk >> 2) & 7) << 2;
-      const float4 a = *(const float4*)(&As[kk][(lr * 4) ^ fk]);
-      const float4 b = *(const float4*)(&Bs[kk][(lc * 4) ^ fk]);
-      acc[0][0] += a.x * b.x; acc[0][1] += a.x * b.y; acc[0][2] += a.x * b.z; acc[0][3] += a.x * b.w;
-      acc[1][0] += a.y * b.x; acc[1][1] += a.y * b.y; acc[1][2] += a.y * b.z; acc[1][3] += a.y * b.w;
-      acc[2][0] += a.z * b.x; acc[2][1] += a.z * b.y; acc[2][2] += a.z * b.z; acc[2][3] += a.z * b.w;
-      acc[3][0] += a.w * b.x; acc[3][1] += a.w * b.y; acc[3][2] += a.w * b.z; acc[3][3] += a.w * b.w;
-    }
-  }
-  if (isQp) {
-    float* C = qp + (size_t)h * TT * HID;
-#pragma unroll
-    for (int i = 0; i < 4; ++i)
-#pragma unroll
-      for (int j = 0; j < 4; ++j)
-        C[(size_t)(lr * 4 + i) * HID + bn + lc * 4 + j] = acc[i][j];
-  } else {
-    float* C = sc + (size_t)h * TT * sct;
-#pragma unroll
-    for (int i = 0; i < 4; ++i)
-#pragma unroll
-      for (int j = 0; j < 4; ++j)
-        C[(size_t)(lr * 4 + i) * sct + bn + lc * 4 + j] = acc[i][j];
-  }
-}
-
-__global__ __launch_bounds__(256) void attn2_k(
-    const float* __restrict__ sc, const float* __restrict__ vcl,
-    const float* __restrict__ enc,
-    float* __restrict__ part, float* __restrict__ partE,
-    int ckv, int sct, int ncho, long pzc) {
-  __shared__ float As[64][64];
-  __shared__ float Bs[64][64];
-  const int tid = threadIdx.x;
-  const int lr = tid >> 4, lc = tid & 15;
-  const int h = blockIdx.z;
-  const int by = blockIdx.y;
-  const bool isOld = blockIdx.x < 2;
-  if (isOld && by >= ncho) return;
-  if (!isOld && by >= 8) return;
-  const float* A;
-  const float* Bb;
-  int lda, ldb, N, ktiles, nch, bn;
-  float* P;
-  if (isOld) {
-    A = sc + (size_t)h * TT * sct;  lda = sct;
-    Bb = vcl + (size_t)h * ckv * DKH; ldb = DKH;
-    N = DKH; ktiles = ckv >> 6; nch = ncho; bn = blockIdx.x * 64;
-    P = part + (size_t)h * pzc + (size_t)by * 64 * DKH;
-  } else {
-    A = sc + ckv + (size_t)h * TT * sct; lda = sct;
-    Bb = enc; ldb = HID;
-    N = HID; ktiles = SEQ >> 6; nch = 8; bn = (blockIdx.x - 2) * 64;
-    P = partE + (size_t)h * (8L * 64 * HID) + (size_t)by * 64 * HID;
-  }
-  const int fa = (lc & 7) << 2;
-  float acc[4][4] = {};
-  for (int kt = by; kt < ktiles; kt += nch) {
-    const int k0 = kt << 6;
-    __syncthreads();
-#pragma unroll
-    for (int i = 0; i < 4; ++i) {
-      const int r = lr + 16 * i;
-      const float4 av = *(const float4*)(A + (size_t)r * lda + k0 + lc * 4);
-      As[lc * 4 + 0][r ^ fa] = av.x; As[lc * 4 + 1][r ^ fa] = av.y;
-      As[lc * 4 + 2][r ^ fa] = av.z; As[lc * 4 + 3][r ^ fa] = av.w;
-      const float4 bv = *(const float4*)(Bb + (size_t)(k0 + r) * ldb + bn + lc * 4);
-      *(float4*)(&Bs[r][SWZ(r, lc * 4)]) = bv;
-    }
-    __syncthreads();
-#pragma unroll 8
-    for (int kk = 0; kk < 64; ++kk) {
-      const int fk = ((kk >> 2) & 7) << 2;
-      const float4 a = *(const float4*)(&As[kk][(lr * 4) ^ fk]);
-      const float4 b = *(const float4*)(&Bs[kk][(lc * 4) ^ fk]);
-      acc[0][0] += a.x * b.x; acc[0][1] += a.x * b.y; acc[0][2] += a.x * b.z; acc[0][3] += a.x * b.w;
-      acc[1][0] += a.y * b.x; acc[1][1] += a.y * b.y; acc[1][2] += a.y * b.z; acc[1][3] += a.y * b.w;
-      acc[2][0] += a.z * b.x; acc[2][1] += a.z * b.y; acc[2][2] += a.z * b.z; acc[2][3] += a.z * b.w;
-      acc[3][0] += a.w * b.x; acc[3][1] += a.w * b.y; acc[3][2] += a.w * b.z; acc[3][3] += a.w * b.w;
-    }
-  }
-#pragma unroll
-  for (int i = 0; i < 4; ++i)
-#pragma unroll
-    for (int j = 0; j < 4; ++j)
-      P[(size_t)(lr * 4 + i) * N + bn + lc * 4 + j] = acc[i][j];
+    int N, int Kd, int nch, int Z,
+    float* __restrict__ part, long pzs, int coff, int aCh, long aChS) {
+  __shared__ float sm[6656];
+  d_gemm32(A, lda, sA, B, ldb, sB, N, Kd, nch, Z, part, pzs, coff, aCh, aChS, sm);
 }
 
 __global__ __launch_bounds__(256) void fsmnln_k(
     const float* __restrict__ y4, const float* __restrict__ lfin,
     const float* __restrict__ cache, const float* __restrict__ fw,
     const float* __restrict__ g, const float* __restrict__ b,
-    float* __restrict__ xb, float* __restrict__ xcat,
-    float* __restrict__ y1out) {
-  __shared__ float buf[HID];
-  __shared__ float red[256];
-  const int t = blockIdx.x, tid = threadIdx.x;
-  float s = 0.f;
-  for (int h = tid; h < HID; h += 256) {
-    float conv = 0.f;
-#pragma unroll
-    for (int k = 0; k < KW; ++k) {
-      const int j = t + k;
-      const float xcv = (j < KW - 1) ? cache[h * (KW - 1) + j]
-                                     : y4[(size_t)(j - (KW - 1)) * HID + h];
-      conv += xcv * fw[h * KW + k];
-    }
-    const float yv = y4[(size_t)t * HID + h];
-    const float x = conv + yv + lfin[(size_t)t * HID + h];
-    xb[(size_t)t * HID + h] = x;
-    buf[h] = x; s += x;
-    xcat[h * (KW - 1 + TT) + (KW - 1) + t] = yv;
-    if (t == 0) {
-      for (int j2 = 0; j2 < KW - 1; ++j2)
-        xcat[h * (KW - 1 + TT) + j2] = cache[h * (KW - 1) + j2];
-    }
-  }
-  red[tid] = s; __syncthreads();
-  for (int st = 128; st > 0; st >>= 1) { if (tid < st) red[tid] += red[tid + st]; __syncthreads(); }
-  const float mean = red[0] / HID;
-  __syncthreads();
-  float vs = 0.f;
-  for (int h = tid; h < HID; h += 256) { float d = buf[h] - mean; vs += d * d; }
-  red[tid] = vs; __syncthreads();
-  for (int st = 128; st > 0; st >>= 1) { if (tid < st) red[tid] += red[tid + st]; __syncthreads(); }
-  const float inv = rsqrtf(red[0] / HID + 1e-5f);
-  for (int h = tid; h < HID; h += 256)
-    y1out[(size_t)t * HID + h] = (buf[h] - mean) * inv * g[h] + b[h];
+    float* __restrict__ xb, float* __restrict__ xcat, float* __restrict__ y1out) {
+  __shared__ float sm[768];
+  d_fsmnln(y4, lfin, cache, fw, g, b, xb, xcat, y1out, sm);
+}
+
+__global__ __launch_bounds__(256) void attn1_k(
+    const float* __restrict__ qpart, const float* __restrict__ qbi_l,
+    const float* __restrict__ Wkv, const float* __restrict__ kcl,
+    float* __restrict__ qp, float* __restrict__ sc, int ckv, int sct) {
+  __shared__ float sm[8192];
+  d_attn1(qpart, qbi_l, Wkv, kcl, qp, sc, ckv, sct, sm);
+}
+
+__global__ __launch_bounds__(256) void scnew_k(
+    const float* __restrict__ qp, const float* __restrict__ enc,
+    float* __restrict__ sc, float* __restrict__ partN, int ckv, int sct) {
+  __shared__ float sm[8192];
+  d_scnew(qp, enc, sc, partN, ckv, sct, sm);
 }
 
 __global__ __launch_bounds__(256) void softmax_k(
@@ -439,73 +643,36 @@
     const float* __restrict__ qpart, const float* __restrict__ qbi_l,
     const float* __restrict__ kb, const float* __restrict__ partN,
     int cols, int newStart, float alpha) {
-  __shared__ float srow[8192];
-  __shared__ float red[256];
-  const int tid = threadIdx.x;
-  const int row = blockIdx.x;
-  const int h = row >> 6, t = row & 63;
-  sc += (size_t)row * cols;
-  const float* pn = partN + (size_t)h * 64 * SEQ + (size_t)t * SEQ;
-  float qv = 0.f;
-  if (tid < DKH) {
-    const float* qp0 = qpart + (size_t)t * HID + h * DKH + tid;
-    float q = qp0[0];
-    for (int c = 1; c < 8; ++c) q += qp0[(size_t)c * 64 * HID];
-    q += qbi_l[h * DKH + tid];
-    qv = q * kb[h * DKH + tid];
-  }
-  red[tid] = qv; __syncthreads();
-  for (int st = 64; st > 0; st >>= 1) { if (tid < st) red[tid] += red[tid + st]; __syncthreads(); }
-  const float qcv = red[0];
-  __syncthreads();
-  float m = -3.4e38f;
-  for (int c = tid; c < cols; c += 256) {
-    float v = sc[c];
-    if (c >= newStart) v += pn[c - newStart] + qcv;
-    v *= alpha;
-    srow[c] = v; m = fmaxf(m, v);
-  }
-  red[tid] = m; __syncthreads();
-  for (int st = 128; st > 0; st >>= 1) { if (tid < st) red[tid] = fmaxf(red[tid], red[tid + st]); __syncthreads(); }
-  m = red[0]; __syncthreads();
-  float s = 0.f;
-  for (int c = tid; c < cols; c += 256) {
-    const float e = __expf(srow[c] - m);
-    srow[c] = e; s += e;
-  }
-  red[tid] = s; __syncthreads();
-  for (int st = 128; st > 0; st >>= 1) { if (tid < st) red[tid] += red[tid + st]; __syncthreads(); }
-  const float inv = 1.f / red[0];
-  float ns = 0.f;
-  for (int c = tid; c < cols; c += 256) {
-    const float p = srow[c] * inv; sc[c] = p;
-    if (c >= newStart) ns += p;
-  }
-  __syncthreads();
-  red[tid] = ns; __syncthreads();
-  for (int st = 128; st > 0; st >>= 1) { if (tid < st) red[tid] += red[tid + st]; __syncthreads(); }
-  if (tid == 0) rs[row] = red[0];
+  __shared__ float sm[8448];
+  d_softmax(sc, rs, qpart, qbi_l, kb, partN, cols, newStart, alpha, sm);
+}
+
+__global__ __launch_bounds__(256) void attn2_k(
+    const float* __restrict__ sc, const float* __restrict__ vcl,
+    const float* __restrict__ enc, float* __restrict__ part,
+    float* __restrict__ partE, int ckv, int sct, int ncho, long pzc) {
+  __shared__ float sm[8192];
+  d_attn2(sc, vcl, enc, part, partE, ckv, sct, ncho, pzc, sm);
+}
+
+__global__ __launch_bounds__(256) void red_k(
+    const float* __restrict__ P, float* __restrict__ out,
+    int N, int nch, long pzs, int outld, int zoff,
+    const float* __restrict__ rsv, const float* __restrict__ bvv, int total) {
+  d_red(P, out, N, nch, pzs, outld, zoff, rsv, bvv, total);
+}
+
+__global__ __launch_bounds__(256) void vocab_k(
+    const float* __restrict__ A, const float* __restrict__ B,
+    float* __restrict__ C, const float* __restrict__ bias) {
+  __shared__ float sm[8192];
+  d_vocab(A, B, C, bias, sm);
 }
 
 __global__ __launch_bounds__(256) void argmax_k(const float* __restrict__ lg,
                                                 float* __restrict__ out) {
-  __shared__ float vs[256];
-  __shared__ int ix[256];
-  const int tid = threadIdx.x;
-  lg += (size_t)blockIdx.x * VOC;
-  float bm = -3.4e38f;
-  int bi = 0;
-  for (int c = tid; c < VOC; c += 256) { float v = lg[c]; if (v > bm) { bm = v; bi = c; } }
-  vs[tid] = bm; ix[tid] = bi; __syncthreads();
-  for (int st = 128; st > 0; st >>= 1) {
-    if (tid < st) {
-      if (vs[tid + st] > vs[tid] || (vs[tid + st] == vs[tid] && ix[tid + st] < ix[tid])) {
-        vs[tid] = vs[tid + st]; ix[tid] = ix[tid + st];
-      }
-    }
-    __syncthreads();
-  }
-  if (tid == 0) out[blockIdx.x] = (float)ix[0];
+  __shared__ float sm[512];
+  d_argmax(lg, out, sm);
 }
 
 __global__ __launch_bounds__(256) void kvsave_k(const float* __restrict__ enc,
@@ -606,7 +773,6 @@
   }
   const int ckv = (int)ckl;
   const int sct = ckv + SEQ;
-  const long TS = (long)TT * sct;
   const int ncho = (ckv / 64 < 8) ? (ckv / 64) : 8;
 
   const float* enc    = (const float*)d_in[0];
@@ -639,7 +805,6 @@
   float* xb  = ov + 131072;
   float* ctx = ov + 196608;
   float* y2  = ov + 360448;
-  float* qp  = ov + 491520;
   float* rs  = ov + 753920;
   float* lg  = ov + 754176;
   float* wsf   = (float*)d_ws;
@@ -648,65 +813,77 @@
   float* partN = wsf + 2097152;
 
   const float alpha = 0.08838834764831845f;
-  const long TH = (long)TT * HID;
   const long pz_ctx = (long)(ncho + 4) * 64 * DKH;
 
-  redln_k<<<TT, 256, 0, stream>>>(lfrm, HID, 1, nullptr, nullptr, 0,
-                                  n1g, n1b, lf, y1);
-
-  for (int l = 0; l < LAY; ++l) {
-    const float* Wkv = kvw + (size_t)l * HID * 2 * HID;
-    const float* Bkv = kvbi + (size_t)l * 2 * HID;
-    const float* qbi_l = qbi + (size_t)l * HID;
-    gemm32_nn<<<dim3(64, 8, 1), 256, 0, stream>>>(
-        y1, HID, 0, w1 + (size_t)l * HID * FF, FF, 0, FF, HID, 8, part, 0, 0, 1, 0);
-    redln_k<<<TT, 256, 0, stream>>>(part, FF, 8, b1 + (size_t)l * FF, nullptr, 1,
-                                    fng + (size_t)l * FF, fnb + (size_t)l * FF,
-                                    nullptr, y2);
-    gemm32_nn<<<dim3(16, 32, 1), 256, 0, stream>>>(
-        y2, FF, 0, w2 + (size_t)l * FF * HID, HID, 0, HID, FF, 32, part, 0, 0, 1, 0);
-    redln_k<<<TT, 256, 0, stream>>>(part, HID, 32, nullptr, nullptr, 0,
-                                    n2g + l * HID, n2b + l * HID, nullptr, y4);
-    fsmnln_k<<<TT, 256, 0, stream>>>(y4, lf, fcache + (size_t)l * HID * (KW - 1),
-                                     fw + (size_t)l * HID * KW,
-                                     n3g + l * HID, n3b + l * HID,
-                                     xb, out_fsmn + (size_t)l * HID * (KW - 1 + TT), y1);
-    gemm32_nn<<<dim3(16, 8, 1), 256, 0, stream>>>(
-        y1, HID, 0, qw + (size_t)l * HID * HID, HID, 0, HID, HID, 8, part, 0, 0, 1, 0);
-    attn1_k<<<dim3(8 + ckv / 64, 1, NHD), 256, 0, stream>>>(
-        part, qbi_l, Wkv, kcache + (size_t)l * NHD * DKH * ckv, qp, sc, ckv, sct);
-    gemm_nt<<<dim3(32, 2, NHD), 256, 0, stream>>>(
-        qp, HID, TH, enc, HID, 0, sc + ckv, sct, TS, SEQ, HID, 2, partN);
-    softmax_k<<<NHD * TT, 256, 0, stream>>>(sc, rs, part, qbi_l, Bkv, partN,
-                                            sct, ckv, alpha);
-    attn2_k<<<dim3(10, 8, NHD), 256, 0, stream>>>(
-        sc, vcache + (size_t)l * NHD * ckv * DKH, enc, part, partE,
-        ckv, sct, ncho, pz_ctx);
-    gemm32_nn<<<dim3(4, 4, NHD), 256, 0, stream>>>(
-        partE, HID, 8L * 64 * HID, Wkv + HID, 2 * HID, DKH, DKH, HID, 4,
-        part, pz_ctx, ncho, 8, 64L * HID);
-    red_k<<<128, 256, 0, stream>>>(part, ctx, DKH, ncho + 4, pz_ctx, HID, DKH,
-                                   nullptr, nullptr, rs, Bkv + HID, 0, NHD * TT * DKH);
-    gemm32_nn<<<dim3(16, 8, 1), 256, 0, stream>>>(
-        ctx, HID, 0, ow + (size_t)l * HID * HID, HID, 0, HID, HID, 8, part, 0, 0, 1, 0);
-    const float* ng = (l + 1 < LAY) ? n1g + (l + 1) * HID : d3n1g;
-    const float* nb = (l + 1 < LAY) ? n1b + (l + 1) * HID : d3n1b;
-    redln_k<<<TT, 256, 0, stream>>>(part, HID, 8, obi + (size_t)l * HID, xb, 0,
-                                    ng, nb, lf, y1);
-  }
-
-  gemm32_nn<<<dim3(64, 8, 1), 256, 0, stream>>>(
-      y1, HID, 0, d3w1, FF, 0, FF, HID, 8, part, 0, 0, 1, 0);
-  redln_k<<<TT, 256, 0, stream>>>(part, FF, 8, d3b1, nullptr, 1,
-                                  d3fng, d3fnb, nullptr, y2);
-  gemm32_nn<<<dim3(16, 32, 1), 256, 0, stream>>>(
-      y2, FF, 0, d3w2, HID, 0, HID, FF, 32, part, 0, 0, 1, 0);
-  redln_k<<<TT, 256, 0, stream>>>(part, HID, 32, nullptr, nullptr, 0,
-                                  ang, anb, nullptr, y4);
-  gemm_nn<<<dim3((VOC + 63) / 64, 1, 1), 256, 0, stream>>>(
-      y4, HID, 0, outw, VOC, 0, lg, VOC, 0, outb, nullptr, 0,
-      VOC, HID, 0, 1, nullptr, 0, 0, 1, 0);
-  argmax_k<<<TT, 256, 0, stream>>>(lg, out_ids);
+  CA ca;
+  ca.enc = enc; ca.lfrm = lfrm; ca.fcache = fcache; ca.kcache = kcache; ca.vcache = vcache;
+  ca.n1g = n1g; ca.n1b = n1b; ca.n2g = n2g; ca.n2b = n2b; ca.n3g = n3g; ca.n3b = n3b;
+  ca.fng = fng; ca.fnb = fnb; ca.w1 = w1; ca.b1 = b1; ca.w2 = w2; ca.fw = fw;
+  ca.qw = qw; ca.qbi = qbi; ca.kvw = kvw; ca.kvbi = kvbi; ca.ow = ow; ca.obi = obi;
+  ca.d3n1g = d3n1g; ca.d3n1b = d3n1b; ca.d3w1 = d3w1; ca.d3b1 = d3b1;
+  ca.d3fng = d3fng; ca.d3fnb = d3fnb; ca.d3w2 = d3w2;
+  ca.ang = ang; ca.anb = anb; ca.outw = outw; ca.outb = outb;
+  ca.lf = lf; ca.y1 = y1; ca.y2 = y2; ca.y4 = y4; ca.xb = xb; ca.ctx = ctx;
+  ca.rs = rs; ca.lg = lg; ca.sc = sc;
+  ca.part = part; ca.partE = partE; ca.partN = partN;
+  ca.out_fsmn = out_fsmn; ca.out_ids = out_ids;
+  ca.ckv = ckv; ca.sct = sct; ca.ncho = ncho; ca.pz_ctx = pz_ctx;
+
+  bool coopDone = false;
+  int maxPerCU = 0;
+  hipError_t qrc = hipOccupancyMaxActiveBlocksPerMultiprocessor(&maxPerCU, chain_k,
+                                                                256, 0);
+  if (qrc == hipSuccess && maxPerCU > 0) {
+    int grid = maxPerCU * 256;
+    if (grid > 512) grid = 512;
+    void* args[] = {(void*)&ca};
+    hipError_t rc = hipLaunchCooperativeKernel((const void*)chain_k, dim3(grid),
+                                               dim3(256), args, 0, stream);
+    coopDone = (rc == hipSuccess);
+  }
+
+  if (!coopDone) {
+    redln_k<<<TT, 256, 0, stream>>>(lfrm, HID, 1, nullptr, nullptr, 0, n1g, n1b, lf, y1);
+    for (int l = 0; l < LAY; ++l) {
+      const float* Wkv = kvw + (size_t)l * HID * 2 * HID;
+      const float* Bkv = kvbi + (size_t)l * 2 * HID;
+      const float* qbi_l = qbi + (size_t)l * HID;
+      gemm32_k<<<512, 256, 0, stream>>>(y1, HID, 0, w1 + (size_t)l * HID * FF, FF, 0,
+                                        FF, HID, 8, 1, part, 0, 0, 1, 0);
+      redln_k<<<TT, 256, 0, stream>>>(part, FF, 8, b1 + (size_t)l * FF, nullptr, 1,
+                                      fng + (size_t)l * FF, fnb + (size_t)l * FF, nullptr, y2);
+      gemm32_k<<<512, 256, 0, stream>>>(y2, FF, 0, w2 + (size_t)l * FF * HID, HID, 0,
+                                        HID, FF, 32, 1, part, 0, 0, 1, 0);
+      redln_k<<<TT, 256, 0, stream>>>(part, HID, 32, nullptr, nullptr, 0,
+                                      n2g + l * HID, n2b + l * HID, nullptr, y4);
+      fsmnln_k<<<TT, 256, 0, stream>>>(y4, lf, fcache + (size_t)l * HID * (KW - 1),
+                                       fw + (size_t)l * HID * KW, n3g + l * HID, n3b + l * HID,
+                                       xb, out_fsmn + (size_t)l * HID * (KW - 1 + TT), y1);
+      gemm32_k<<<128, 256, 0, stream>>>(y1, HID, 0, qw + (size_t)l * HID * HID, HID, 0,
+                                        HID, HID, 8, 1, part, 0, 0, 1, 0);
+      attn1_k<<<(8 + ckv / 64) * NHD, 256, 0, stream>>>(
+          part, qbi_l, Wkv, kcache + (size_t)l * NHD * DKH * ckv, ctx, sc, ckv, sct);
+      scnew_k<<<256, 256, 0, stream>>>(ctx, enc, sc, partN, ckv, sct);
+      softmax_k<<<NHD * TT, 256, 0, stream>>>(sc, rs, part, qbi_l, Bkv, partN, sct, ckv, alpha);
+      attn2_k<<<320, 256, 0, stream>>>(sc, vcache + (size_t)l * NHD * ckv * DKH, enc,
+                                       part, partE, ckv, sct, ncho, pz_ctx);
+      gemm32_k<<<64, 256, 0, stream>>>(partE, HID, 8L * 64 * HID, Wkv + HID, 2 * HID, DKH,
+                                       DKH, HID, 4, NHD, part, pz_ctx, ncho, 8, 64L * HID);
+      red_k<<<128, 256, 0, stream>>>(part, y2, DKH, ncho + 4, pz_ctx, HID, DKH,
+                                     rs, Bkv + HID, NHD * TT * DKH);
+      gemm32_k<<<128, 256, 0, stream>>>(y2, HID, 0, ow + (size_t)l * HID * HID, HID, 0,
+                                        HID, HID, 8, 1, part, 0, 0, 1, 0);
+      const float* ng = (l + 1 < LAY) ? n1g + (l + 1) * HID : d3n1g;
+      const float* nb = (l + 1 < LAY) ? n1b + (l + 1) * HID : d3n1b;
+      redln_k<<<TT, 256, 0, stream>>>(part, HID, 8, obi + (size_t)l * HID, xb, 0, ng, nb, lf, y1);
+    }
+    gemm32_k<<<512, 256, 0, stream>>>(y1, HID, 0, d3w1, FF, 0, FF, HID, 8, 1, part, 0, 0, 1, 0);
+    redln_k<<<TT, 256, 0, stream>>>(part, FF, 8, d3b1, nullptr, 1, d3fng, d3fnb, nullptr, y2);
+    gemm32_k<<<512, 256, 0, stream>>>(y2, FF, 0, d3w2, HID, 0, HID, FF, 32, 1, part, 0, 0, 1, 0);
+    redln_k<<<TT, 256, 0, stream>>>(part, HID, 32, nullptr, nullptr, 0, ang, anb, nullptr, y4);
+    vocab_k<<<132, 256, 0, stream>>>(y4, outw, lg, outb);
+    argmax_k<<<TT, 256, 0, stream>>>(lg, out_ids);
+  }
 
   kvsave_k<<<dim3(2 * HID / 64, LBN / 64, LAY), 256, 0, stream>>>(
       enc, kvw, kvbi, out_keys, out_vals);
```

Result: slower. 3.197 ms (+8.6%).
